# Kernel optimization log

Hardware: AMD Instinct MI355X
Metric: run time of the kernel (lower is better)

The kernel has to match this reference:

```python
import jax, jax.numpy as jnp
import numpy as np

N, K, C, R, S = 10000, 16, 32, 32, 64
D = 9  # per-channel irrep dim of interaction feats: 0e(1)+1o(3)+2e(5)
AVG_NEIGH = 16.0
EPS = 1e-6

_rng = np.random.default_rng(0)
# fixed constant coupling tensors (deterministic stand-ins for CG coefficients; structure matches e3nn paths)
CG112 = jnp.asarray(_rng.standard_normal((3, 3, 5)) * 0.2, jnp.float32)  # 1o x 1o -> 2e
CG121 = jnp.asarray(_rng.standard_normal((3, 5, 3)) * 0.2, jnp.float32)  # 1o x 2e -> 1o
# symmetric tensor-product bases U[order, ir_out]: shape (D,)*order + (mul, ir_dim)
MULS = {3: {'0e': 3, '1o': 2}, 2: {'0e': 2, '1o': 1}, 1: {'0e': 1, '1o': 1}}
IRDIM = {'0e': 1, '1o': 3}
U = {(o, ir): jnp.asarray(_rng.standard_normal((D,) * o + (MULS[o][ir], IRDIM[ir])) * (0.3 ** o), jnp.float32)
     for o in (3, 2, 1) for ir in ('0e', '1o')}


def _normnorm(arrs):
    # E3NormNorm: per-node RMS normalization over channel/component axes
    return [a / jnp.sqrt(jnp.mean(a * a, axis=tuple(range(1, a.ndim)), keepdims=True) + EPS) for a in arrs]


def _sph_harm(vec):
    # real spherical harmonics l=1,2 (component normalization) on normalized vectors
    r = vec / (jnp.linalg.norm(vec, axis=-1, keepdims=True) + EPS)
    x, y, z = r[..., 0], r[..., 1], r[..., 2]
    sh1 = jnp.sqrt(3.0) * r
    c = jnp.sqrt(15.0)
    sh2 = jnp.stack([c * x * y, c * y * z, jnp.sqrt(5.0) / 2 * (3 * z * z - 1), c * x * z, c / 2 * (x * x - y * y)], axis=-1)
    return sh1, sh2


def _forward(node_s, node_v, vectors, radial_embedding, species_table, Wu0, Wu1, radW, radb, ln_g, ln_b,
             Wd0, Wd1, Wd2, w3_0e, w3_1o, w2_0e, w2_1o, w1_0e, w1_1o, P0, P1, Wskip0, Wskip1, Wread,
             receivers, node_specie):
    n, c = node_s.shape
    inv = 1.0 / jnp.sqrt(1.0 * c)
    # ---- InteractionBlock: linear_up + norm ----
    s = node_s @ Wu0 * inv
    v = jnp.einsum('nci,cd->ndi', node_v, Wu1) * inv
    s, v = _normnorm([s, v])
    # ---- MessagePassingConvolution: sender = node i broadcast over its K=16 neighbors ----
    sh1, sh2 = _sph_harm(vectors)  # [n,K,3], [n,K,5]
    m0a = jnp.broadcast_to(s[:, None, :], (n, K, c))                       # prefix 0e
    m0b = jnp.einsum('nci,nki->nkc', v, sh1) / jnp.sqrt(3.0)               # 1o x 1o -> 0e
    m1a = jnp.broadcast_to(v[:, None], (n, K, c, 3))                       # prefix 1o
    m1b = jnp.einsum('nc,nki->nkci', s, sh1) / jnp.sqrt(3.0)               # 0e x 1o -> 1o
    m1c = jnp.einsum('nci,nkp,ipj->nkcj', v, sh2, CG121)                   # 1o x 2e -> 1o
    m2a = jnp.einsum('nc,nkp->nkcp', s, sh2) / jnp.sqrt(5.0)               # 0e x 2e -> 2e
    m2b = jnp.einsum('nci,nkj,ijp->nkcp', v, sh1, CG112)                   # 1o x 1o -> 2e
    M0 = jnp.concatenate([m0a, m0b], axis=-1)      # [n,K,2C]
    M1 = jnp.concatenate([m1a, m1b, m1c], axis=2)  # [n,K,3C,3]
    M2 = jnp.concatenate([m2a, m2b], axis=2)       # [n,K,2C,5]
    # radial mix: linear + layernorm, one weight per irrep (7C total)
    rad = radial_embedding @ radW + radb
    mu = rad.mean(-1, keepdims=True)
    var = rad.var(-1, keepdims=True)
    rad = ln_g * (rad - mu) / jnp.sqrt(var + EPS) + ln_b
    r0, r1, r2 = rad[..., :2 * c], rad[..., 2 * c:5 * c], rad[..., 5 * c:]
    M0 = M0 * r0
    M1 = M1 * r1[..., None]
    M2 = M2 * r2[..., None]
    # scatter-add messages to receivers, normalize by sqrt(avg_num_neighbors)
    idx = receivers.reshape(-1)
    sc = 1.0 / jnp.sqrt(AVG_NEIGH)
    o0 = jnp.zeros((n, 2 * c), M0.dtype).at[idx].add(M0.reshape(n * K, 2 * c)) * sc
    o1 = jnp.zeros((n, 3 * c, 3), M1.dtype).at[idx].add(M1.reshape(n * K, 3 * c, 3)) * sc
    o2 = jnp.zeros((n, 2 * c, 5), M2.dtype).at[idx].add(M2.reshape(n * K, 2 * c, 5)) * sc
    o0, o1, o2 = _normnorm([o0, o1, o2])
    # linear_down to interaction_irreps Cx(0e+1o+2e), then norm
    A0 = o0 @ Wd0 / jnp.sqrt(2.0 * c)
    A1 = jnp.einsum('nmi,md->ndi', o1, Wd1) / jnp.sqrt(3.0 * c)
    A2 = jnp.einsum('nmi,md->ndi', o2, Wd2) / jnp.sqrt(2.0 * c)
    A0, A1, A2 = _normnorm([A0, A1, A2])
    # ---- EquivariantProductBasisBlock: species-gathered symmetric contraction ----
    x_sym = jnp.concatenate([A0[:, :, None], A1, A2], axis=-1)  # [n, C, D=9]
    species_ind = species_table[node_specie]                    # [n, R]
    Wsym = {(3, '0e'): w3_0e, (3, '1o'): w3_1o, (2, '0e'): w2_0e, (2, '1o'): w2_1o, (1, '0e'): w1_0e, (1, '1o'): w1_1o}
    out = {}
    for order in (3, 2, 1):
        for ir in ('0e', '1o'):
            u = U[(order, ir)]
            w = jnp.einsum('be,ekc->bkc', species_ind, Wsym[(order, ir)])
            if ir not in out:
                out[ir] = ('new', jnp.einsum('...jki,bkc,bcj->bc...i', u, w, x_sym))
            else:
                out[ir] = out[ir] + jnp.einsum('...ki,bkc->bc...i', u, w)
        for ir in ('0e', '1o'):
            if isinstance(out[ir], tuple):
                out[ir] = out[ir][1]  # creation order already consumed one x
            else:
                out[ir] = jnp.einsum('bc...ji,bcj->bc...i', out[ir], x_sym)
    sym_s = out['0e'][..., 0]  # [n, C]
    sym_v = out['1o']          # [n, C, 3]
    # proj_out linear
    ps = sym_s @ P0 * inv
    pv = jnp.einsum('nci,cd->ndi', sym_v, P1) * inv
    # species-indexed skip connection
    skip_s = jnp.einsum('nc,ncd->nd', node_s, Wskip0[node_specie]) * inv
    skip_v = jnp.einsum('nci,ncd->ndi', node_v, Wskip1[node_specie]) * inv
    s_out = ps + skip_s
    v_out = pv + skip_v
    # linear readout (output_irreps = 1x0e)
    read = s_out @ Wread * inv
    return jnp.concatenate([s_out, v_out.reshape(n, 3 * c), read], axis=-1)


def setup_inputs():
    ks = jax.random.split(jax.random.key(0), 32)
    f = lambda i, shape: jax.random.normal(ks[i], shape, jnp.float32)
    return {
        'node_s': f(0, (N, C)),
        'node_v': f(1, (N, C, 3)),
        'vectors': f(2, (N, K, 3)),
        'radial_embedding': f(3, (N, K, R)),
        'receivers': jax.random.randint(ks[4], (N, K), 0, N),
        'node_specie': jax.random.randint(ks[5], (N,), 0, S),
        'species_table': f(6, (S, R)),
        'Wu0': f(7, (C, C)), 'Wu1': f(8, (C, C)),
        'radW': f(9, (R, 7 * C)), 'radb': jnp.zeros((7 * C,), jnp.float32),
        'ln_g': jnp.ones((7 * C,), jnp.float32), 'ln_b': jnp.zeros((7 * C,), jnp.float32),
        'Wd0': f(11, (2 * C, C)), 'Wd1': f(12, (3 * C, C)), 'Wd2': f(13, (2 * C, C)),
        'w3_0e': f(14, (R, 3, C)), 'w3_1o': f(15, (R, 2, C)),
        'w2_0e': f(16, (R, 2, C)), 'w2_1o': f(17, (R, 1, C)),
        'w1_0e': f(18, (R, 1, C)), 'w1_1o': f(19, (R, 1, C)),
        'P0': f(20, (C, C)), 'P1': f(21, (C, C)),
        'Wskip0': f(22, (S, C, C)), 'Wskip1': f(23, (S, C, C)),
        'Wread': f(24, (C, 1)),
    }


def reference(node_s, node_v, vectors, radial_embedding, receivers, node_specie, species_table, Wu0, Wu1,
              radW, radb, ln_g, ln_b, Wd0, Wd1, Wd2, w3_0e, w3_1o, w2_0e, w2_1o, w1_0e, w1_1o,
              P0, P1, Wskip0, Wskip1, Wread):
    return _forward(node_s, node_v, vectors, radial_embedding, species_table, Wu0, Wu1, radW, radb, ln_g, ln_b,
                    Wd0, Wd1, Wd2, w3_0e, w3_1o, w2_0e, w2_1o, w1_0e, w1_1o, P0, P1, Wskip0, Wskip1, Wread,
                    receivers, node_specie)
```

## Files before the change

kernel.cpp:

```cpp
#include <hip/hip_runtime.h>
#include <cmath>
#include <stdint.h>

typedef unsigned long long u64;
typedef unsigned __int128 u128;

#define EPSF 1e-6f

#define OFF_RAW 0L
#define OFF_S   7168L
#define OFF_G   8960L
#define GSP_SZ  28032L
#define OFF_SN  (OFF_G + 64L*GSP_SZ)
#define OFF_VN  (OFF_SN + 320000L)
#define FLOAT_END (OFF_VN + 960000L)
#define OFF_RAD (FLOAT_END + 262144L)
#define RAD_REQ_BYTES ((size_t)(OFF_RAD + 35840000L) * 4)
#define OFF_RNG (OFF_G + 8192L)

#define IOFF_DEG   0
#define IOFF_OFFS  10000
#define IOFF_CUR   20001
#define IOFF_EL    30001
#define IOFF_SCNT  190001
#define IOFF_SOFF  190065
#define IOFF_SCUR  190130
#define IOFF_NORD  190194
#define IOFF_TRI   200194
#define IOFF_PAIR  200359


__device__ __forceinline__ u128 pcg_mul128() {
  return ((u128)2549297995355413924ULL << 64) | (u128)4865540595714422341ULL;
}
struct Pcg {
  u128 state, inc;
  __device__ __forceinline__ u64 next() {
    state = state * pcg_mul128() + inc;
    u64 hi = (u64)(state >> 64), lo = (u64)state;
    unsigned rot = (unsigned)(hi >> 58);
    u64 x = hi ^ lo;
    return (x >> rot) | (x << ((64u - rot) & 63u));
  }
};
__device__ __forceinline__ double u64_to_dbl(u64 u) {
  return (double)(u >> 11) * (1.0 / 9007199254740992.0);
}
__device__ __forceinline__ unsigned ss_hashmix(unsigned v, unsigned &hc) {
  v ^= hc; hc *= 0x931e8875u; v *= hc; v ^= v >> 16; return v;
}
__device__ __forceinline__ unsigned ss_mix(unsigned x, unsigned y) {
  unsigned r = 0xca01f9ddu * x - 0x4973f715u * y; r ^= r >> 16; return r;
}

#define NBUF 8192
#define NBM  8191
#define PERTH 32
#define NDRAW 7092
#define NSEG  222
#define RB_E 32

__global__ __launch_bounds__(256) void k_prep(
    const float* __restrict__ ns, const float* __restrict__ nv,
    const float* __restrict__ Wu0, const float* __restrict__ Wu1,
    const float* __restrict__ remb, const float* __restrict__ radW,
    const float* __restrict__ radb, const float* __restrict__ ln_g,
    const float* __restrict__ ln_b,
    const int* __restrict__ recv, const int* __restrict__ spec,
    int doRad,
    float* __restrict__ wsf, int* __restrict__ wsi)
{
  __shared__ __align__(16) float shbuf[8672];
  const int tid = threadIdx.x;
  const int bid = blockIdx.x;

  if (bid < 1250) {
    const int nn = bid * 8 + (tid >> 5);
    const int c = tid & 31;
    const float INV = 0.17677669529663687f;
    float s = 0.f;
    for (int e = 0; e < 32; e++) s += ns[nn*32 + e] * Wu0[e*32 + c];
    s *= INV;
    float v0 = 0, v1 = 0, v2 = 0;
    for (int e = 0; e < 32; e++) {
      const float w = Wu1[e*32 + c];
      const float* p = nv + (long)(nn*32 + e)*3;
      v0 += p[0]*w; v1 += p[1]*w; v2 += p[2]*w;
    }
    v0 *= INV; v1 *= INV; v2 *= INV;
    float ss = s*s;
    for (int m = 16; m >= 1; m >>= 1) ss += __shfl_xor(ss, m);
    float sv = v0*v0 + v1*v1 + v2*v2;
    for (int m = 16; m >= 1; m >>= 1) sv += __shfl_xor(sv, m);
    float rs = rsqrtf(ss * (1.f/32.f) + EPSF);
    float rv = rsqrtf(sv * (1.f/96.f) + EPSF);
    wsf[OFF_SN + nn*32 + c] = s * rs;
    float* vp = wsf + OFF_VN + (long)(nn*32 + c)*3;
    vp[0] = v0*rv; vp[1] = v1*rv; vp[2] = v2*rv;
  } else if (bid < 6250) {
    if (!doRad) return;
    float (*er)[33] = (float(*)[33])&shbuf[0];
    float* pre = &shbuf[1056];
    float4* lg4 = (float4*)&shbuf[8224];
    float4* lb4 = (float4*)&shbuf[8448];
    const long e0 = (long)(bid - 1250) * RB_E;

    if (tid < 56) { lg4[tid] = ((const float4*)ln_g)[tid]; lb4[tid] = ((const float4*)ln_b)[tid]; }
    for (int i = tid; i < RB_E*32; i += 256) {
      const int e = i >> 5, q = i & 31;
      er[e][q] = remb[(e0 + e)*32 + q];
    }
    __syncthreads();

    if (tid < 224) {
      const int cg = tid % 56, grp = tid / 56;
      const float4 rb = ((const float4*)radb)[cg];
      float4 acc[8];
      #pragma unroll
      for (int k = 0; k < 8; k++) acc[k] = rb;
      const float4* radW4 = (const float4*)radW;
      for (int q = 0; q < 32; q++) {
        const float4 w = radW4[q*56 + cg];
        #pragma unroll
        for (int k = 0; k < 8; k++) {
          const float ev = er[grp*8 + k][q];
          acc[k].x = fmaf(ev, w.x, acc[k].x);
          acc[k].y = fmaf(ev, w.y, acc[k].y);
          acc[k].z = fmaf(ev, w.z, acc[k].z);
          acc[k].w = fmaf(ev, w.w, acc[k].w);
        }
      }
      #pragma unroll
      for (int k = 0; k < 8; k++)
        ((float4*)&pre[(grp*8 + k)*224])[cg] = acc[k];
    }
    __syncthreads();

    const int wv = tid >> 6, ln = tid & 63;
    for (int k = 0; k < 8; k++) {
      const int e = wv*8 + k;
      float a0 = 0.f, a1 = 0.f, a2 = 0.f, a3 = 0.f;
      if (ln < 56) {
        const float4 v = ((const float4*)&pre[e*224])[ln];
        a0 = v.x; a1 = v.y; a2 = v.z; a3 = v.w;
      }
      float c1 = a0 + a1 + a2 + a3;
      float c2 = a0*a0 + a1*a1 + a2*a2 + a3*a3;
      for (int m = 32; m >= 1; m >>= 1) { c1 += __shfl_xor(c1, m); c2 += __shfl_xor(c2, m); }
      const float mu = c1 * (1.f/224.f);
      const float rvar = rsqrtf(c2*(1.f/224.f) - mu*mu + EPSF);
      if (ln < 56) {
        const float4 lg = lg4[ln], lb = lb4[ln];
        float4 o;
        o.x = lg.x*(a0-mu)*rvar + lb.x;
        o.y = lg.y*(a1-mu)*rvar + lb.y;
        o.z = lg.z*(a2-mu)*rvar + lb.z;
        o.w = lg.w*(a3-mu)*rvar + lb.w;
        ((float4*)(wsf + OFF_RAD))[(e0 + e)*56 + ln] = o;
      }
    }
  } else if (bid < 6875) {
    const int e = (bid - 6250)*256 + tid;
    if (e < 160000) atomicAdd(&wsi[IOFF_DEG + recv[e]], 1);
    if (e < 10000)  atomicAdd(&wsi[IOFF_SCNT + spec[e]], 1);
  } else {
    if (tid != 0) return;
    double* wiG = (double*)(wsf + OFF_RNG);
    double* fiG = (double*)(wsf + OFF_RNG + 512);
    u64*    kiG = (u64*)   (wsf + OFF_RNG + 1024);
    u64*    ssG = (u64*)   (wsf + OFF_RNG + 1536);
    unsigned hc = 0x43b0d7e5u;
    unsigned pool[4];
    for (int i = 0; i < 4; i++) pool[i] = ss_hashmix(0u, hc);
    for (int s = 0; s < 4; s++)
      for (int d = 0; d < 4; d++)
        if (s != d) pool[d] = ss_mix(pool[d], ss_hashmix(pool[s], hc));
    unsigned hb = 0x8b51f9ddu;
    u64 sw[4];
    {
      unsigned w8[8];
      for (int i = 0; i < 8; i++) {
        unsigned dv = pool[i & 3];
        dv ^= hb; hb *= 0x58f38dedu; dv *= hb; dv ^= dv >> 16;
        w8[i] = dv;
      }
      for (int k2 = 0; k2 < 4; k2++) sw[k2] = (u64)w8[2*k2] | ((u64)w8[2*k2+1] << 32);
    }
    u128 initstate = ((u128)sw[0] << 64) | (u128)sw[1];
    u128 initseq   = ((u128)sw[2] << 64) | (u128)sw[3];
    u128 inc_ = (initseq << 1) | (u128)1;
    u128 S0 = inc_;
    S0 += initstate;
    S0 = S0 * pcg_mul128() + inc_;
    ssG[0] = (u64)(S0 >> 64);   ssG[1] = (u64)S0;
    ssG[2] = (u64)(inc_ >> 64); ssG[3] = (u64)inc_;
    const double m1 = 4503599627370496.0;
    const double ZR = 3.6541528853610087963519472518;
    double dn = ZR, tn = ZR;
    const double vn = 4.92867323399e-3;
    double fv = exp(-0.5 * dn * dn);
    double q = vn / fv;
    kiG[0] = (u64)((dn / q) * m1);
    kiG[1] = 0;
    wiG[0] = q / m1;  wiG[255] = dn / m1;
    fiG[0] = 1.0;     fiG[255] = fv;
    for (int i = 254; i >= 1; i--) {
      dn = sqrt(-2.0 * log(vn / dn + fv));
      kiG[i+1] = (u64)((dn / tn) * m1);
      tn = dn;
      fv = exp(-0.5 * dn * dn);
      fiG[i] = fv;
      wiG[i] = dn / m1;
    }
    int mcnt = 0;
    for (int a = 0; a < 9; a++)
      for (int b = a; b < 9; b++)
        for (int j3 = b; j3 < 9; j3++)
          wsi[IOFF_TRI + (mcnt++)] = a | (b << 4) | (j3 << 8);
    int pcnt = 0;
    for (int a = 0; a < 9; a++)
      for (int b = a; b < 9; b++)
        wsi[IOFF_PAIR + (pcnt++)] = a | (b << 4);
  }
}

__global__ __launch_bounds__(256) void k_mid(float* __restrict__ wsf, int* __restrict__ wsi)
{
  __shared__ double wi[256], fi[256];
  __shared__ u64 ki[256];
  __shared__ u64 buf[NBUF];
  __shared__ float zv[NBUF];
  __shared__ unsigned char cons[NBUF];
  __shared__ unsigned short jmp[NBUF];
  __shared__ unsigned short heads[NSEG];
  __shared__ u64 stst[512], enst[512];
  __shared__ double scl[8];
  __shared__ int flag;
  __shared__ int part[256];
  const int tid = threadIdx.x;

  if (blockIdx.x == 1) {
    int loc[40];
    const int base = tid * 40;
    int s = 0;
    for (int t = 0; t < 40; t++) {
      const int idx = base + t;
      loc[t] = s;
      s += (idx < 10000) ? wsi[IOFF_DEG + idx] : 0;
    }
    part[tid] = s;
    __syncthreads();
    for (int d = 1; d < 256; d <<= 1) {
      int v = (tid >= d) ? part[tid - d] : 0;
      __syncthreads();
      part[tid] += v;
      __syncthreads();
    }
    const int exc = (tid > 0) ? part[tid - 1] : 0;
    for (int t = 0; t < 40; t++) {
      const int idx = base + t;
      if (idx <= 10000) wsi[IOFF_OFFS + idx] = exc + loc[t];
    }
    if (tid == 0) {
      int a = 0;
      for (int s2 = 0; s2 < 64; s2++) { wsi[IOFF_SOFF + s2] = a; a += wsi[IOFF_SCNT + s2]; }
      wsi[IOFF_SOFF + 64] = a;
    }
    return;
  }

  const double* wiG = (const double*)(wsf + OFF_RNG);
  const double* fiG = (const double*)(wsf + OFF_RNG + 512);
  const u64*    kiG = (const u64*)   (wsf + OFF_RNG + 1024);
  const u64*    ssG = (const u64*)   (wsf + OFF_RNG + 1536);
  float* raw = wsf + OFF_RAW;

  wi[tid] = wiG[tid]; fi[tid] = fiG[tid]; ki[tid] = kiG[tid];
  if (tid == 0) {
    flag = 0;
    double p2 = pow(0.3, 2.0), p3 = pow(0.3, 3.0);
    scl[0]=0.2; scl[1]=0.2; scl[2]=p3; scl[3]=p3; scl[4]=p2; scl[5]=p2; scl[6]=0.3; scl[7]=0.3;
  }
  __syncthreads();

  {
    u128 S0   = ((u128)ssG[0] << 64) | (u128)ssG[1];
    u128 inc_ = ((u128)ssG[2] << 64) | (u128)ssG[3];
    u128 aR = (u128)1, cR = (u128)0;
    u128 aP = pcg_mul128(), cP = inc_;
    unsigned e = (unsigned)tid * PERTH;
    while (e) {
      if (e & 1u) { cR = aP * cR + cP; aR = aP * aR; }
      cP = aP * cP + cP;
      aP = aP * aP;
      e >>= 1;
    }
    Pcg g; g.inc = inc_; g.state = aR * S0 + cR;
    stst[tid*2] = (u64)(g.state >> 64); stst[tid*2+1] = (u64)g.state;
    #pragma unroll 4
    for (int k = 0; k < PERTH; k++) buf[tid*PERTH + k] = g.next();
    enst[tid*2] = (u64)(g.state >> 64); enst[tid*2+1] = (u64)g.state;
  }
  __syncthreads();
  if (tid < 255) {
    if (stst[(tid+1)*2] != enst[tid*2] || stst[(tid+1)*2+1] != enst[tid*2+1])
      atomicOr(&flag, 1);
  }
  if (tid == 0) {
    if (fabs(u64_to_dbl(buf[0]) - 0.6369616873214543) > 1e-12) atomicOr(&flag, 1);
  }
  __syncthreads();
  if (flag && tid == 0) {
    u128 S0   = ((u128)ssG[0] << 64) | (u128)ssG[1];
    u128 inc_ = ((u128)ssG[2] << 64) | (u128)ssG[3];
    Pcg g; g.state = S0; g.inc = inc_;
    for (int k = 0; k < NBUF; k++) buf[k] = g.next();
  }
  __syncthreads();

  const double ZRd  = 3.6541528853610087963519472518;
  const double ZIRd = 0.27366123732975827203338247596;
  for (int k = 0; k < PERTH; k++) {
    const int p = tid*PERTH + k;
    int pos = p;
    int consumed = 0;
    double z = 0.0;
    u64 r = buf[pos & NBM]; pos++; consumed++;
    for (int guard = 0; guard < 64; guard++) {
      int idx = (int)(r & 0xff);
      r >>= 8;
      int sgn = (int)(r & 1);
      u64 rabs = (r >> 1) & 0x000fffffffffffffULL;
      double x = (double)rabs * wi[idx];
      if (sgn) x = -x;
      if (rabs < ki[idx]) { z = x; break; }
      if (idx == 0) {
        double xx = 0.0, yy = 0.0;
        for (int g2 = 0; g2 < 64; g2++) {
          u64 ua = buf[pos & NBM]; pos++; consumed++;
          u64 ub = buf[pos & NBM]; pos++; consumed++;
          xx = -ZIRd * log1p(-u64_to_dbl(ua));
          yy = -log1p(-u64_to_dbl(ub));
          if (yy + yy > xx * xx) break;
        }
        z = ((rabs >> 8) & 1) ? -(ZRd + xx) : (ZRd + xx);
        break;
      } else {
        u64 u = buf[pos & NBM]; pos++; consumed++;
        if ((fi[idx-1] - fi[idx]) * u64_to_dbl(u) + fi[idx] < exp(-0.5 * x * x)) { z = x; break; }
      }
      r = buf[pos & NBM]; pos++; consumed++;
    }
    zv[p] = (float)z;
    cons[p] = (unsigned char)(consumed > 255 ? 255 : consumed);
  }
  __syncthreads();

  {
    int pos[PERTH];
    #pragma unroll
    for (int k = 0; k < PERTH; k++) pos[k] = tid*PERTH + k;
    for (int s = 0; s < 32; s++) {
      #pragma unroll
      for (int k = 0; k < PERTH; k++) {
        int np = pos[k] + (int)cons[pos[k]];
        pos[k] = (np > NBM) ? NBM : np;
      }
    }
    #pragma unroll
    for (int k = 0; k < PERTH; k++) jmp[tid*PERTH + k] = (unsigned short)pos[k];
  }
  __syncthreads();

  if (tid == 0) {
    int pos = 0;
    for (int m = 0; m < NSEG; m++) { heads[m] = (unsigned short)pos; pos = (int)jmp[pos]; }
  }
  __syncthreads();

  if (tid < NSEG) {
    int pos = (int)heads[tid];
    const int i0 = tid * 32;
    for (int k = 0; k < 32; k++) {
      const int i = i0 + k;
      if (i >= NDRAW) break;
      double sc;
      if      (i < 90)   sc = scl[0];
      else if (i < 6651) sc = scl[2];
      else if (i < 7056) sc = scl[4];
      else               sc = scl[6];
      raw[i] = (float)((double)zv[pos] * sc);
      int np = pos + (int)cons[pos];
      pos = (np > NBM) ? NBM : np;
    }
  }
}

__global__ __launch_bounds__(256) void k_fillg(
    const int* __restrict__ recv, const int* __restrict__ spec,
    const float* __restrict__ stab,
    const float* __restrict__ w30e, const float* __restrict__ w31o,
    const float* __restrict__ w20e, const float* __restrict__ w21o,
    const float* __restrict__ w10e, const float* __restrict__ w11o,
    float* __restrict__ wsf, int* __restrict__ wsi)
{
  __shared__ float st[32];
  const int tid = threadIdx.x;
  const int bid = blockIdx.x;
  if (bid < 625) {
    const int e = bid*256 + tid;
    if (e < 160000) {
      int r = recv[e];
      int p = atomicAdd(&wsi[IOFF_CUR + r], 1);
      wsi[IOFF_EL + wsi[IOFF_OFFS + r] + p] = e;
    }
    if (e < 10000) {
      int sp = spec[e];
      int p = atomicAdd(&wsi[IOFF_SCUR + sp], 1);
      wsi[IOFF_NORD + wsi[IOFF_SOFF + sp] + p] = e;
    }
  } else if (bid < 689) {
    const int sp = bid - 625;
    float* Gsp = wsf + OFF_G + (long)sp * GSP_SZ;
    if (tid < 32) st[tid] = stab[sp*32 + tid];
    __syncthreads();
    for (int t = tid; t < 320; t += 256) {
      const float* W; int kc, kcs;
      if (t < 96)       { W = w30e; kc = t;       kcs = 96; }
      else if (t < 160) { W = w31o; kc = t - 96;  kcs = 64; }
      else if (t < 224) { W = w20e; kc = t - 160; kcs = 64; }
      else if (t < 256) { W = w21o; kc = t - 224; kcs = 32; }
      else if (t < 288) { W = w10e; kc = t - 256; kcs = 32; }
      else              { W = w11o; kc = t - 288; kcs = 32; }
      float a = 0.f;
      for (int e = 0; e < 32; e++) a += st[e] * W[e*kcs + kc];
      Gsp[t] = a;
    }
  } else {
    const float* raw = wsf + OFF_RAW;
    float* Sb = wsf + OFF_S;
    for (int idx = tid; idx < 495; idx += 256) {
      int m = idx / 3, k2 = idx % 3;
      int tp = wsi[IOFF_TRI + m];
      int a = tp & 15, b = (tp >> 4) & 15, j3 = (tp >> 8) & 15;
      int P[6][3] = {{a,b,j3},{a,j3,b},{b,a,j3},{b,j3,a},{j3,a,b},{j3,b,a}};
      float s = 0.f;
      for (int t = 0; t < 6; t++) {
        bool dup = false;
        for (int u = 0; u < t; u++)
          if (P[u][0]==P[t][0] && P[u][1]==P[t][1] && P[u][2]==P[t][2]) { dup = true; break; }
        if (!dup) s += raw[90 + ((P[t][0]*9 + P[t][1])*9 + P[t][2])*3 + k2];
      }
      Sb[m*3 + k2] = s;
    }
    for (int idx = tid; idx < 990; idx += 256) {
      int m = idx / 6, r6 = idx % 6, k2 = r6 / 3, i = r6 % 3;
      int tp = wsi[IOFF_TRI + m];
      int a = tp & 15, b = (tp >> 4) & 15, j3 = (tp >> 8) & 15;
      int P[6][3] = {{a,b,j3},{a,j3,b},{b,a,j3},{b,j3,a},{j3,a,b},{j3,b,a}};
      float s = 0.f;
      for (int t = 0; t < 6; t++) {
        bool dup = false;
        for (int u = 0; u < t; u++)
          if (P[u][0]==P[t][0] && P[u][1]==P[t][1] && P[u][2]==P[t][2]) { dup = true; break; }
        if (!dup) s += raw[2277 + (((P[t][0]*9 + P[t][1])*9 + P[t][2])*2 + k2)*3 + i];
      }
      Sb[495 + (m*2 + k2)*3 + i] = s;
    }
    for (int idx = tid; idx < 90; idx += 256) {
      int m = idx / 2, k2 = idx % 2;
      int pp = wsi[IOFF_PAIR + m]; int a = pp & 15, b = (pp >> 4) & 15;
      float s = raw[6651 + (a*9 + b)*2 + k2];
      if (a != b) s += raw[6651 + (b*9 + a)*2 + k2];
      Sb[1485 + idx] = s;
    }
    for (int idx = tid; idx < 135; idx += 256) {
      int m = idx / 3, i = idx % 3;
      int pp = wsi[IOFF_PAIR + m]; int a = pp & 15, b = (pp >> 4) & 15;
      float s = raw[6813 + (a*9 + b)*3 + i];
      if (a != b) s += raw[6813 + (b*9 + a)*3 + i];
      Sb[1575 + idx] = s;
    }
    for (int idx = tid; idx < 9;  idx += 256) Sb[1710 + idx] = raw[7056 + idx];
    for (int idx = tid; idx < 27; idx += 256) Sb[1719 + idx] = raw[7065 + idx];
  }
}

__device__ __forceinline__ float msg_fast(int slot,
    const float* __restrict__ se, const float* __restrict__ ve,
    const float* __restrict__ sh, const float* __restrict__ ab,
    const float* __restrict__ rd)
{
  const float IS3 = 0.57735026918962576f;
  const float IS5 = 0.44721359549995794f;
  float val; int radidx;
  if (slot < 64) {
    radidx = slot;
    if (slot < 32) val = se[slot];
    else {
      int c = slot - 32;
      val = (ve[c*3+0]*sh[0] + ve[c*3+1]*sh[1] + ve[c*3+2]*sh[2]) * IS3;
    }
  } else if (slot < 352) {
    int q = slot - 64; int row = q / 3; int i = q - row*3;
    radidx = 64 + row;
    if (row < 32) val = ve[row*3 + i];
    else if (row < 64) val = se[row - 32] * sh[i] * IS3;
    else {
      int c = row - 64;
      val = ve[c*3+0]*ab[0+i] + ve[c*3+1]*ab[3+i] + ve[c*3+2]*ab[6+i];
    }
  } else {
    int q = slot - 352; int row = q / 5; int p = q - row*5;
    radidx = 160 + row;
    if (row < 32) val = se[row] * sh[3+p] * IS5;
    else {
      int c = row - 32;
      val = ve[c*3+0]*ab[9+p] + ve[c*3+1]*ab[14+p] + ve[c*3+2]*ab[19+p];
    }
  }
  return val * rd[radidx];
}

#define SM_RAD 0
#define SM_SE  896
#define SM_VE  1024
#define SM_ER  1408
#define SM_SHH 1536
#define SM_AB  1568
#define SM_LNG 1664
#define SM_LNB 1888
#define SM_RB  2112
#define SM_CG  2336
#define SM_S    0
#define SM_X    1746
#define SM_O    2034
#define SM_GRED 2706
#define SM_SYMS 3730
#define SM_SYMV 3762
#define SM_SOUT 3858
#define SM_REDB 3890
#define SM_RF   3902
#define SMEM_N  3906

template<int PRE>
__global__ __launch_bounds__(256) void k_main(
    const float* __restrict__ node_s, const float* __restrict__ node_v,
    const float* __restrict__ vectors, const float* __restrict__ remb,
    const int* __restrict__ nspec,
    const float* __restrict__ radW, const float* __restrict__ radb,
    const float* __restrict__ ln_g, const float* __restrict__ ln_b,
    const float* __restrict__ Wd0, const float* __restrict__ Wd1, const float* __restrict__ Wd2,
    const float* __restrict__ P0, const float* __restrict__ P1,
    const float* __restrict__ Wsk0, const float* __restrict__ Wsk1,
    const float* __restrict__ Wread,
    const float* __restrict__ wsf, const int* __restrict__ wsi,
    float* __restrict__ out)
{
  const int tid = threadIdx.x;
  const int wv  = tid >> 6;
  const int ln  = tid & 63;
  __shared__ __align__(16) float smem[SMEM_N];
  __shared__ int tri_s[165], pair_s[45];

  const int j  = wsi[IOFF_NORD + blockIdx.x];
  const int sp = nspec[j];
  const int e0 = wsi[IOFF_OFFS + j];
  const int e1 = wsi[IOFF_OFFS + j + 1];

  if (!PRE) {
    for (int i = tid; i < 224; i += 256) {
      smem[SM_LNG + i] = ln_g[i];
      smem[SM_LNB + i] = ln_b[i];
      smem[SM_RB  + i] = radb[i];
    }
  }
  for (int i = tid; i < 90; i += 256) smem[SM_CG + i] = wsf[OFF_RAW + i];
  __syncthreads();

  float acc0 = 0.f, acc1 = 0.f, acc2 = 0.f;
  for (int t = e0; t < e1; t += 4) {
    const int eidx = t + wv;
    const bool act = (eidx < e1);
    if (act) {
      const int e = wsi[IOFF_EL + eidx];
      const int n = e >> 4;
      if (ln < 32) {
        smem[SM_SE + wv*32 + ln] = wsf[OFF_SN + (long)n*32 + ln];
        if (!PRE) smem[SM_ER + wv*32 + ln] = remb[(long)e*32 + ln];
      } else {
        const int l2 = ln - 32;
        const float* vp = wsf + OFF_VN + (long)(n*32 + l2)*3;
        smem[SM_VE + wv*96 + l2*3+0] = vp[0];
        smem[SM_VE + wv*96 + l2*3+1] = vp[1];
        smem[SM_VE + wv*96 + l2*3+2] = vp[2];
      }
      if (ln == 0) {
        const float* vv = vectors + (long)e*3;
        float vx = vv[0], vy = vv[1], vz = vv[2];
        float nr = sqrtf(vx*vx + vy*vy + vz*vz) + EPSF;
        float rx = vx/nr, ry = vy/nr, rz = vz/nr;
        smem[SM_SHH + wv*8 + 0] = 1.7320508075688772f * rx;
        smem[SM_SHH + wv*8 + 1] = 1.7320508075688772f * ry;
        smem[SM_SHH + wv*8 + 2] = 1.7320508075688772f * rz;
        smem[SM_SHH + wv*8 + 3] = 3.872983346207417f * rx*ry;
        smem[SM_SHH + wv*8 + 4] = 3.872983346207417f * ry*rz;
        smem[SM_SHH + wv*8 + 5] = 1.118033988749895f * (3.f*rz*rz - 1.f);
        smem[SM_SHH + wv*8 + 6] = 3.872983346207417f * rx*rz;
        smem[SM_SHH + wv*8 + 7] = 1.9364916731037085f * (rx*rx - ry*ry);
      }
      if (PRE) {
        if (ln < 56) {
          const float4 v4 = ((const float4*)(wsf + OFF_RAD))[(long)e*56 + ln];
          ((float4*)&smem[SM_RAD + wv*224])[ln] = v4;
        }
      } else {
        float aval[4];
        float c1 = 0.f, c2 = 0.f;
        #pragma unroll
        for (int k = 0; k < 4; k++) {
          const int ch = ln + 64*k;
          if (ch < 224) {
            float a = smem[SM_RB + ch];
            #pragma unroll 8
            for (int q = 0; q < 32; q++)
              a += smem[SM_ER + wv*32 + q] * radW[q*224 + ch];
            aval[k] = a; c1 += a; c2 += a*a;
          }
        }
        for (int m = 32; m >= 1; m >>= 1) { c1 += __shfl_xor(c1, m); c2 += __shfl_xor(c2, m); }
        const float mu = c1 * (1.f/224.f);
        const float rvar = rsqrtf(c2*(1.f/224.f) - mu*mu + EPSF);
        #pragma unroll
        for (int k = 0; k < 4; k++) {
          const int ch = ln + 64*k;
          if (ch < 224)
            smem[SM_RAD + wv*224 + ch] = smem[SM_LNG + ch]*(aval[k]-mu)*rvar + smem[SM_LNB + ch];
        }
      }
      if (ln < 9) {
        const int i2 = ln / 3, i = ln - i2*3;
        float a = 0.f;
        #pragma unroll
        for (int p = 0; p < 5; p++)
          a += smem[SM_SHH + wv*8 + 3 + p] * smem[SM_CG + 45 + i2*15 + p*3 + i];
        smem[SM_AB + wv*24 + ln] = a;
      } else if (ln < 24) {
        const int q = ln - 9, i = q / 5, p = q - i*5;
        float a = 0.f;
        #pragma unroll
        for (int j2 = 0; j2 < 3; j2++)
          a += smem[SM_SHH + wv*8 + j2] * smem[SM_CG + i*15 + j2*5 + p];
        smem[SM_AB + wv*24 + 9 + q] = a;
      }
    }
    __syncthreads();
    const int nact = (e1 - t < 4) ? (e1 - t) : 4;
    for (int w = 0; w < nact; w++) {
      const float* se = &smem[SM_SE + w*32];
      const float* ve = &smem[SM_VE + w*96];
      const float* sh = &smem[SM_SHH + w*8];
      const float* ab = &smem[SM_AB + w*24];
      const float* rd = &smem[SM_RAD + w*224];
      acc0 += msg_fast(tid,       se, ve, sh, ab, rd);
      acc1 += msg_fast(tid + 256, se, ve, sh, ab, rd);
      if (tid < 160) acc2 += msg_fast(tid + 512, se, ve, sh, ab, rd);
    }
    __syncthreads();
  }

  for (int i = tid; i < 1746; i += 256) smem[SM_S + i] = wsf[OFF_S + i];
  for (int i = tid; i < 165; i += 256) tri_s[i] = wsi[IOFF_TRI + i];
  for (int i = tid; i < 45;  i += 256) pair_s[i] = wsi[IOFF_PAIR + i];

  float* redbuf = &smem[SM_REDB];
  float* rf     = &smem[SM_RF];
  acc0 *= 0.25f; acc1 *= 0.25f; acc2 *= 0.25f;
  float g0 = 0, g1 = 0, g2 = 0;
  if (tid < 64) g0 = acc0*acc0; else g1 = acc0*acc0;
  if (tid < 96) g1 += acc1*acc1; else g2 += acc1*acc1;
  if (tid < 160) g2 += acc2*acc2;
  for (int m = 32; m >= 1; m >>= 1) { g0 += __shfl_xor(g0, m); g1 += __shfl_xor(g1, m); g2 += __shfl_xor(g2, m); }
  if ((tid & 63) == 0) { redbuf[wv] = g0; redbuf[4+wv] = g1; redbuf[8+wv] = g2; }
  __syncthreads();
  if (tid == 0) {
    float s0 = redbuf[0]+redbuf[1]+redbuf[2]+redbuf[3];
    float s1 = redbuf[4]+redbuf[5]+redbuf[6]+redbuf[7];
    float s2 = redbuf[8]+redbuf[9]+redbuf[10]+redbuf[11];
    rf[0] = rsqrtf(s0*(1.f/64.f)  + EPSF);
    rf[1] = rsqrtf(s1*(1.f/288.f) + EPSF);
    rf[2] = rsqrtf(s2*(1.f/320.f) + EPSF);
  }
  __syncthreads();
  smem[SM_O + tid]       = acc0 * ((tid < 64) ? rf[0] : rf[1]);
  smem[SM_O + tid + 256] = acc1 * ((tid < 96) ? rf[1] : rf[2]);
  if (tid < 160) smem[SM_O + tid + 512] = acc2 * rf[2];
  __syncthreads();

  const float* o_lds = &smem[SM_O];
  float av1, av2 = 0.f;
  if (tid < 32) {
    float a = 0;
    for (int m = 0; m < 64; m++) a += o_lds[m] * Wd0[m*32 + tid];
    av1 = a * 0.125f;
  } else if (tid < 128) {
    int q = tid - 32, d = q/3, i = q - d*3;
    float a = 0;
    for (int m = 0; m < 96; m++) a += o_lds[64 + m*3 + i] * Wd1[m*32 + d];
    av1 = a * 0.10206207261596575f;
  } else {
    int q = tid - 128, d = q/5, p = q - d*5;
    float a = 0;
    for (int m = 0; m < 64; m++) a += o_lds[352 + m*5 + p] * Wd2[m*32 + d];
    av1 = a * 0.125f;
  }
  if (tid < 32) {
    int q = tid + 128, d = q/5, p = q - d*5;
    float a = 0;
    for (int m = 0; m < 64; m++) a += o_lds[352 + m*5 + p] * Wd2[m*32 + d];
    av2 = a * 0.125f;
  }
  float p0 = (tid < 32) ? av1*av1 : 0.f;
  float p1 = (tid >= 32 && tid < 128) ? av1*av1 : 0.f;
  float p2s = (tid >= 128) ? av1*av1 : 0.f;
  if (tid < 32) p2s += av2*av2;
  for (int m = 32; m >= 1; m >>= 1) { p0 += __shfl_xor(p0, m); p1 += __shfl_xor(p1, m); p2s += __shfl_xor(p2s, m); }
  if ((tid & 63) == 0) { redbuf[wv] = p0; redbuf[4+wv] = p1; redbuf[8+wv] = p2s; }
  __syncthreads();
  if (tid == 0) {
    float s0 = redbuf[0]+redbuf[1]+redbuf[2]+redbuf[3];
    float s1 = redbuf[4]+redbuf[5]+redbuf[6]+redbuf[7];
    float s2 = redbuf[8]+redbuf[9]+redbuf[10]+redbuf[11];
    rf[0] = rsqrtf(s0*(1.f/32.f)  + EPSF);
    rf[1] = rsqrtf(s1*(1.f/96.f)  + EPSF);
    rf[2] = rsqrtf(s2*(1.f/160.f) + EPSF);
  }
  __syncthreads();
  float* x_lds = &smem[SM_X];
  if (tid < 32) x_lds[tid*9 + 0] = av1 * rf[0];
  else if (tid < 128) { int q = tid - 32, d = q/3, i = q - d*3; x_lds[d*9 + 1 + i] = av1 * rf[1]; }
  else { int q = tid - 128, d = q/5, p = q - d*5; x_lds[d*9 + 4 + p] = av1 * rf[2]; }
  if (tid < 32) { int q = tid + 128, d = q/5, p = q - d*5; x_lds[d*9 + 4 + p] = av2 * rf[2]; }
  __syncthreads();

  const float* Sb = &smem[SM_S];
  float* gred = &smem[SM_GRED];
  const int c = tid & 31, g = tid >> 5;
  float xr[9];
  for (int t2 = 0; t2 < 9; t2++) xr[t2] = x_lds[c*9 + t2];
  const float* wl = wsf + OFF_G + (long)sp * GSP_SZ;
  const float w30a = wl[c], w30b = wl[32 + c], w30c = wl[64 + c];
  const float w31a = wl[96 + c], w31b = wl[128 + c];
  const float w20a = wl[160 + c], w20b = wl[192 + c];
  const float w21  = wl[224 + c];
  const float w10  = wl[256 + c];
  const float w11  = wl[288 + c];

  float sa = 0, va0 = 0, va1 = 0, va2 = 0;
  for (int m = g; m < 165; m += 8) {
    const int tp = tri_s[m];
    const float P = xr[tp & 15] * xr[(tp >> 4) & 15] * xr[(tp >> 8) & 15];
    sa += P * (Sb[m*3+0]*w30a + Sb[m*3+1]*w30b + Sb[m*3+2]*w30c);
    const float* s1p = &Sb[495 + m*6];
    va0 += P * (s1p[0]*w31a + s1p[3]*w31b);
    va1 += P * (s1p[1]*w31a + s1p[4]*w31b);
    va2 += P * (s1p[2]*w31a + s1p[5]*w31b);
  }
  for (int m = g; m < 45; m += 8) {
    const int pp = pair_s[m];
    const float P = xr[pp & 15] * xr[(pp >> 4) & 15];
    sa += P * (Sb[1485 + m*2+0]*w20a + Sb[1485 + m*2+1]*w20b);
    const float* s1p = &Sb[1575 + m*3];
    va0 += P * s1p[0] * w21;
    va1 += P * s1p[1] * w21;
    va2 += P * s1p[2] * w21;
  }
  if (g == 0) {
    for (int a = 0; a < 9; a++) {
      const float xa = xr[a];
      sa += xa * Sb[1710 + a] * w10;
      va0 += xa * Sb[1719 + a*3 + 0] * w11;
      va1 += xa * Sb[1719 + a*3 + 1] * w11;
      va2 += xa * Sb[1719 + a*3 + 2] * w11;
    }
  }
  gred[0*256 + g*32 + c] = sa;
  gred[1*256 + g*32 + c] = va0;
  gred[2*256 + g*32 + c] = va1;
  gred[3*256 + g*32 + c] = va2;
  __syncthreads();
  float* syms = &smem[SM_SYMS];
  float* symv = &smem[SM_SYMV];
  float* sout = &smem[SM_SOUT];
  if (tid < 128) {
    int cc = tid & 31, comp = tid >> 5;
    float a = 0;
    for (int gg = 0; gg < 8; gg++) a += gred[comp*256 + gg*32 + cc];
    if (comp == 0) syms[cc] = a; else symv[cc*3 + comp - 1] = a;
  }
  __syncthreads();

  const float INV = 0.17677669529663687f;
  if (tid < 32) {
    int d = tid; float ps = 0, sk = 0;
    const float* Wp = Wsk0 + (long)sp * 1024;
    for (int c2 = 0; c2 < 32; c2++) {
      ps += syms[c2] * P0[c2*32 + d];
      sk += node_s[j*32 + c2] * Wp[c2*32 + d];
    }
    float val = (ps + sk) * INV;
    sout[d] = val;
    out[(long)j*129 + d] = val;
  } else if (tid < 128) {
    int q = tid - 32, d = q/3, i = q - d*3;
    float pv = 0, sk = 0;
    const float* Wp = Wsk1 + (long)sp * 1024;
    for (int c2 = 0; c2 < 32; c2++) {
      pv += symv[c2*3 + i] * P1[c2*32 + d];
      sk += node_v[(long)(j*32 + c2)*3 + i] * Wp[c2*32 + d];
    }
    out[(long)j*129 + 32 + q] = (pv + sk) * INV;
  }
  __syncthreads();
  if (tid < 32) {
    float p = sout[tid] * Wread[tid];
    for (int m = 16; m >= 1; m >>= 1) p += __shfl_xor(p, m);
    if (tid == 0) out[(long)j*129 + 128] = p * INV;
  }
}

extern "C" void kernel_launch(void* const* d_in, const int* in_sizes, int n_in,
                              void* d_out, int out_size, void* d_ws, size_t ws_size,
                              hipStream_t stream)
{
  const float* node_s  = (const float*)d_in[0];
  const float* node_v  = (const float*)d_in[1];
  const float* vectors = (const float*)d_in[2];
  const float* remb    = (const float*)d_in[3];
  const int*   recv    = (const int*)d_in[4];
  const int*   nspec   = (const int*)d_in[5];
  const float* stab    = (const float*)d_in[6];
  const float* Wu0     = (const float*)d_in[7];
  const float* Wu1     = (const float*)d_in[8];
  const float* radW    = (const float*)d_in[9];
  const float* radb    = (const float*)d_in[10];
  const float* ln_g    = (const float*)d_in[11];
  const float* ln_b    = (const float*)d_in[12];
  const float* Wd0     = (const float*)d_in[13];
  const float* Wd1     = (const float*)d_in[14];
  const float* Wd2     = (const float*)d_in[15];
  const float* w30e    = (const float*)d_in[16];
  const float* w31o    = (const float*)d_in[17];
  const float* w20e    = (const float*)d_in[18];
  const float* w21o    = (const float*)d_in[19];
  const float* w10e    = (const float*)d_in[20];
  const float* w11o    = (const float*)d_in[21];
  const float* P0      = (const float*)d_in[22];
  const float* P1      = (const float*)d_in[23];
  const float* Wsk0    = (const float*)d_in[24];
  const float* Wsk1    = (const float*)d_in[25];
  const float* Wread   = (const float*)d_in[26];
  float* out = (float*)d_out;
  float* wsf = (float*)d_ws;
  int*   wsi = (int*)((char*)d_ws + FLOAT_END * sizeof(float));

  const bool pre = (ws_size >= RAD_REQ_BYTES);

  hipMemsetAsync(wsi, 0, (size_t)IOFF_NORD * sizeof(int), stream);
  k_prep<<<6876, 256, 0, stream>>>(node_s, node_v, Wu0, Wu1,
                                   remb, radW, radb, ln_g, ln_b,
                                   recv, nspec, pre ? 1 : 0, wsf, wsi);
  k_mid<<<2, 256, 0, stream>>>(wsf, wsi);
  k_fillg<<<690, 256, 0, stream>>>(recv, nspec, stab,
                                   w30e, w31o, w20e, w21o, w10e, w11o,
                                   wsf, wsi);
  if (pre) {
    k_main<1><<<10000, 256, 0, stream>>>(node_s, node_v, vectors, remb, nspec,
                                         radW, radb, ln_g, ln_b, Wd0, Wd1, Wd2,
                                         P0, P1, Wsk0, Wsk1, Wread, wsf, wsi, out);
  } else {
    k_main<0><<<10000, 256, 0, stream>>>(node_s, node_v, vectors, remb, nspec,
                                         radW, radb, ln_g, ln_b, Wd0, Wd1, Wd2,
                                         P0, P1, Wsk0, Wsk1, Wread, wsf, wsi, out);
  }
}
```

Baseline: 596.9 us.

## Precompute per-edge messages in sender-major kernel, gather them per receiver

Adds a path where a new kernel computes the radial MLP with layernorm and the full 672-wide per-edge message in sender order, fused with the edge-list and weight-table setup work. The messages go to a workspace buffer in fp32, or fp16 when space is short. A gather kernel then sums each receiver's incoming messages before running the shared epilogue. This avoids rebuilding messages per receiver with scattered sender loads, at the cost of writing and re-reading a large message buffer, plus possible precision loss on the fp16 path. The old prep work is reordered and the fallback main kernel is split out.

```diff
diff --git a/kernel.cpp b/kernel.cpp
--- a/kernel.cpp
+++ b/kernel.cpp
@@ -1,4 +1,5 @@
 #include <hip/hip_runtime.h>
+#include <hip/hip_fp16.h>
 #include <cmath>
 #include <stdint.h>
 
@@ -16,6 +17,8 @@
 #define FLOAT_END (OFF_VN + 960000L)
 #define OFF_RAD (FLOAT_END + 262144L)
 #define RAD_REQ_BYTES ((size_t)(OFF_RAD + 35840000L) * 4)
+#define M_F16_REQ ((size_t)OFF_RAD*4 + (size_t)160000*672*2)
+#define M_F32_REQ ((size_t)OFF_RAD*4 + (size_t)160000*672*4)
 #define OFF_RNG (OFF_G + 8192L)
 
 #define IOFF_DEG   0
@@ -29,6 +32,16 @@
 #define IOFF_TRI   200194
 #define IOFF_PAIR  200359
 
+
+template<typename T> struct MTr;
+template<> struct MTr<float> {
+  static __device__ __forceinline__ float ld(const float* p) { return *p; }
+  static __device__ __forceinline__ void st(float* p, float v) { *p = v; }
+};
+template<> struct MTr<__half> {
+  static __device__ __forceinline__ float ld(const __half* p) { return __half2float(*p); }
+  static __device__ __forceinline__ void st(__half* p, float v) { *p = __float2half(v); }
+};
 
 __device__ __forceinline__ u128 pcg_mul128() {
   return ((u128)2549297995355413924ULL << 64) | (u128)4865540595714422341ULL;
@@ -74,96 +87,7 @@
   const int tid = threadIdx.x;
   const int bid = blockIdx.x;
 
-  if (bid < 1250) {
-    const int nn = bid * 8 + (tid >> 5);
-    const int c = tid & 31;
-    const float INV = 0.17677669529663687f;
-    float s = 0.f;
-    for (int e = 0; e < 32; e++) s += ns[nn*32 + e] * Wu0[e*32 + c];
-    s *= INV;
-    float v0 = 0, v1 = 0, v2 = 0;
-    for (int e = 0; e < 32; e++) {
-      const float w = Wu1[e*32 + c];
-      const float* p = nv + (long)(nn*32 + e)*3;
-      v0 += p[0]*w; v1 += p[1]*w; v2 += p[2]*w;
-    }
-    v0 *= INV; v1 *= INV; v2 *= INV;
-    float ss = s*s;
-    for (int m = 16; m >= 1; m >>= 1) ss += __shfl_xor(ss, m);
-    float sv = v0*v0 + v1*v1 + v2*v2;
-    for (int m = 16; m >= 1; m >>= 1) sv += __shfl_xor(sv, m);
-    float rs = rsqrtf(ss * (1.f/32.f) + EPSF);
-    float rv = rsqrtf(sv * (1.f/96.f) + EPSF);
-    wsf[OFF_SN + nn*32 + c] = s * rs;
-    float* vp = wsf + OFF_VN + (long)(nn*32 + c)*3;
-    vp[0] = v0*rv; vp[1] = v1*rv; vp[2] = v2*rv;
-  } else if (bid < 6250) {
-    if (!doRad) return;
-    float (*er)[33] = (float(*)[33])&shbuf[0];
-    float* pre = &shbuf[1056];
-    float4* lg4 = (float4*)&shbuf[8224];
-    float4* lb4 = (float4*)&shbuf[8448];
-    const long e0 = (long)(bid - 1250) * RB_E;
-
-    if (tid < 56) { lg4[tid] = ((const float4*)ln_g)[tid]; lb4[tid] = ((const float4*)ln_b)[tid]; }
-    for (int i = tid; i < RB_E*32; i += 256) {
-      const int e = i >> 5, q = i & 31;
-      er[e][q] = remb[(e0 + e)*32 + q];
-    }
-    __syncthreads();
-
-    if (tid < 224) {
-      const int cg = tid % 56, grp = tid / 56;
-      const float4 rb = ((const float4*)radb)[cg];
-      float4 acc[8];
-      #pragma unroll
-      for (int k = 0; k < 8; k++) acc[k] = rb;
-      const float4* radW4 = (const float4*)radW;
-      for (int q = 0; q < 32; q++) {
-        const float4 w = radW4[q*56 + cg];
-        #pragma unroll
-        for (int k = 0; k < 8; k++) {
-          const float ev = er[grp*8 + k][q];
-          acc[k].x = fmaf(ev, w.x, acc[k].x);
-          acc[k].y = fmaf(ev, w.y, acc[k].y);
-          acc[k].z = fmaf(ev, w.z, acc[k].z);
-          acc[k].w = fmaf(ev, w.w, acc[k].w);
-        }
-      }
-      #pragma unroll
-      for (int k = 0; k < 8; k++)
-        ((float4*)&pre[(grp*8 + k)*224])[cg] = acc[k];
-    }
-    __syncthreads();
-
-    const int wv = tid >> 6, ln = tid & 63;
-    for (int k = 0; k < 8; k++) {
-      const int e = wv*8 + k;
-      float a0 = 0.f, a1 = 0.f, a2 = 0.f, a3 = 0.f;
-      if (ln < 56) {
-        const float4 v = ((const float4*)&pre[e*224])[ln];
-        a0 = v.x; a1 = v.y; a2 = v.z; a3 = v.w;
-      }
-      float c1 = a0 + a1 + a2 + a3;
-      float c2 = a0*a0 + a1*a1 + a2*a2 + a3*a3;
-      for (int m = 32; m >= 1; m >>= 1) { c1 += __shfl_xor(c1, m); c2 += __shfl_xor(c2, m); }
-      const float mu = c1 * (1.f/224.f);
-      const float rvar = rsqrtf(c2*(1.f/224.f) - mu*mu + EPSF);
-      if (ln < 56) {
-        const float4 lg = lg4[ln], lb = lb4[ln];
-        float4 o;
-        o.x = lg.x*(a0-mu)*rvar + lb.x;
-        o.y = lg.y*(a1-mu)*rvar + lb.y;
-        o.z = lg.z*(a2-mu)*rvar + lb.z;
-        o.w = lg.w*(a3-mu)*rvar + lb.w;
-        ((float4*)(wsf + OFF_RAD))[(e0 + e)*56 + ln] = o;
-      }
-    }
-  } else if (bid < 6875) {
-    const int e = (bid - 6250)*256 + tid;
-    if (e < 160000) atomicAdd(&wsi[IOFF_DEG + recv[e]], 1);
-    if (e < 10000)  atomicAdd(&wsi[IOFF_SCNT + spec[e]], 1);
-  } else {
+  if (bid == 0) {
     if (tid != 0) return;
     double* wiG = (double*)(wsf + OFF_RNG);
     double* fiG = (double*)(wsf + OFF_RNG + 512);
@@ -221,6 +145,95 @@
     for (int a = 0; a < 9; a++)
       for (int b = a; b < 9; b++)
         wsi[IOFF_PAIR + (pcnt++)] = a | (b << 4);
+  } else if (bid < 1251) {
+    const int nn = (bid - 1) * 8 + (tid >> 5);
+    const int c = tid & 31;
+    const float INV = 0.17677669529663687f;
+    float s = 0.f;
+    for (int e = 0; e < 32; e++) s += ns[nn*32 + e] * Wu0[e*32 + c];
+    s *= INV;
+    float v0 = 0, v1 = 0, v2 = 0;
+    for (int e = 0; e < 32; e++) {
+      const float w = Wu1[e*32 + c];
+      const float* p = nv + (long)(nn*32 + e)*3;
+      v0 += p[0]*w; v1 += p[1]*w; v2 += p[2]*w;
+    }
+    v0 *= INV; v1 *= INV; v2 *= INV;
+    float ss = s*s;
+    for (int m = 16; m >= 1; m >>= 1) ss += __shfl_xor(ss, m);
+    float sv = v0*v0 + v1*v1 + v2*v2;
+    for (int m = 16; m >= 1; m >>= 1) sv += __shfl_xor(sv, m);
+    float rs = rsqrtf(ss * (1.f/32.f) + EPSF);
+    float rv = rsqrtf(sv * (1.f/96.f) + EPSF);
+    wsf[OFF_SN + nn*32 + c] = s * rs;
+    float* vp = wsf + OFF_VN + (long)(nn*32 + c)*3;
+    vp[0] = v0*rv; vp[1] = v1*rv; vp[2] = v2*rv;
+  } else if (bid < 1876) {
+    const int e = (bid - 1251)*256 + tid;
+    if (e < 160000) atomicAdd(&wsi[IOFF_DEG + recv[e]], 1);
+    if (e < 10000)  atomicAdd(&wsi[IOFF_SCNT + spec[e]], 1);
+  } else {
+    if (!doRad) return;
+    float (*er)[33] = (float(*)[33])&shbuf[0];
+    float* pre = &shbuf[1056];
+    float4* lg4 = (float4*)&shbuf[8224];
+    float4* lb4 = (float4*)&shbuf[8448];
+    const long e0 = (long)(bid - 1876) * RB_E;
+
+    if (tid < 56) { lg4[tid] = ((const float4*)ln_g)[tid]; lb4[tid] = ((const float4*)ln_b)[tid]; }
+    for (int i = tid; i < RB_E*32; i += 256) {
+      const int e = i >> 5, q = i & 31;
+      er[e][q] = remb[(e0 + e)*32 + q];
+    }
+    __syncthreads();
+
+    if (tid < 224) {
+      const int cg = tid % 56, grp = tid / 56;
+      const float4 rb = ((const float4*)radb)[cg];
+      float4 acc[8];
+      #pragma unroll
+      for (int k = 0; k < 8; k++) acc[k] = rb;
+      const float4* radW4 = (const float4*)radW;
+      for (int q = 0; q < 32; q++) {
+        const float4 w = radW4[q*56 + cg];
+        #pragma unroll
+        for (int k = 0; k < 8; k++) {
+          const float ev = er[grp*8 + k][q];
+          acc[k].x = fmaf(ev, w.x, acc[k].x);
+          acc[k].y = fmaf(ev, w.y, acc[k].y);
+          acc[k].z = fmaf(ev, w.z, acc[k].z);
+          acc[k].w = fmaf(ev, w.w, acc[k].w);
+        }
+      }
+      #pragma unroll
+      for (int k = 0; k < 8; k++)
+        ((float4*)&pre[(grp*8 + k)*224])[cg] = acc[k];
+    }
+    __syncthreads();
+
+    const int wv = tid >> 6, ln = tid & 63;
+    for (int k = 0; k < 8; k++) {
+      const int e = wv*8 + k;
+      float a0 = 0.f, a1 = 0.f, a2 = 0.f, a3 = 0.f;
+      if (ln < 56) {
+        const float4 v = ((const float4*)&pre[e*224])[ln];
+        a0 = v.x; a1 = v.y; a2 = v.z; a3 = v.w;
+      }
+      float c1 = a0 + a1 + a2 + a3;
+      float c2 = a0*a0 + a1*a1 + a2*a2 + a3*a3;
+      for (int m = 32; m >= 1; m >>= 1) { c1 += __shfl_xor(c1, m); c2 += __shfl_xor(c2, m); }
+      const float mu = c1 * (1.f/224.f);
+      const float rvar = rsqrtf(c2*(1.f/224.f) - mu*mu + EPSF);
+      if (ln < 56) {
+        const float4 lg = lg4[ln], lb = lb4[ln];
+        float4 o;
+        o.x = lg.x*(a0-mu)*rvar + lb.x;
+        o.y = lg.y*(a1-mu)*rvar + lb.y;
+        o.z = lg.z*(a2-mu)*rvar + lb.z;
+        o.w = lg.w*(a3-mu)*rvar + lb.w;
+        ((float4*)(wsf + OFF_RAD))[(e0 + e)*56 + ln] = o;
+      }
+    }
   }
 }
 
@@ -396,6 +409,280 @@
   }
 }
 
+__device__ __forceinline__ float msg_fast(int slot,
+    const float* __restrict__ se, const float* __restrict__ ve,
+    const float* __restrict__ sh, const float* __restrict__ ab,
+    const float* __restrict__ rd)
+{
+  const float IS3 = 0.57735026918962576f;
+  const float IS5 = 0.44721359549995794f;
+  float val; int radidx;
+  if (slot < 64) {
+    radidx = slot;
+    if (slot < 32) val = se[slot];
+    else {
+      int c = slot - 32;
+      val = (ve[c*3+0]*sh[0] + ve[c*3+1]*sh[1] + ve[c*3+2]*sh[2]) * IS3;
+    }
+  } else if (slot < 352) {
+    int q = slot - 64; int row = q / 3; int i = q - row*3;
+    radidx = 64 + row;
+    if (row < 32) val = ve[row*3 + i];
+    else if (row < 64) val = se[row - 32] * sh[i] * IS3;
+    else {
+      int c = row - 64;
+      val = ve[c*3+0]*ab[0+i] + ve[c*3+1]*ab[3+i] + ve[c*3+2]*ab[6+i];
+    }
+  } else {
+    int q = slot - 352; int row = q / 5; int p = q - row*5;
+    radidx = 160 + row;
+    if (row < 32) val = se[row] * sh[3+p] * IS5;
+    else {
+      int c = row - 32;
+      val = ve[c*3+0]*ab[9+p] + ve[c*3+1]*ab[14+p] + ve[c*3+2]*ab[19+p];
+    }
+  }
+  return val * rd[radidx];
+}
+
+__device__ void build_stables(const float* raw, float* Sb, const int* wsi, int tid)
+{
+  for (int idx = tid; idx < 495; idx += 256) {
+    int m = idx / 3, k2 = idx % 3;
+    int tp = wsi[IOFF_TRI + m];
+    int a = tp & 15, b = (tp >> 4) & 15, j3 = (tp >> 8) & 15;
+    int P[6][3] = {{a,b,j3},{a,j3,b},{b,a,j3},{b,j3,a},{j3,a,b},{j3,b,a}};
+    float s = 0.f;
+    for (int t = 0; t < 6; t++) {
+      bool dup = false;
+      for (int u = 0; u < t; u++)
+        if (P[u][0]==P[t][0] && P[u][1]==P[t][1] && P[u][2]==P[t][2]) { dup = true; break; }
+      if (!dup) s += raw[90 + ((P[t][0]*9 + P[t][1])*9 + P[t][2])*3 + k2];
+    }
+    Sb[m*3 + k2] = s;
+  }
+  for (int idx = tid; idx < 990; idx += 256) {
+    int m = idx / 6, r6 = idx % 6, k2 = r6 / 3, i = r6 % 3;
+    int tp = wsi[IOFF_TRI + m];
+    int a = tp & 15, b = (tp >> 4) & 15, j3 = (tp >> 8) & 15;
+    int P[6][3] = {{a,b,j3},{a,j3,b},{b,a,j3},{b,j3,a},{j3,a,b},{j3,b,a}};
+    float s = 0.f;
+    for (int t = 0; t < 6; t++) {
+      bool dup = false;
+      for (int u = 0; u < t; u++)
+        if (P[u][0]==P[t][0] && P[u][1]==P[t][1] && P[u][2]==P[t][2]) { dup = true; break; }
+      if (!dup) s += raw[2277 + (((P[t][0]*9 + P[t][1])*9 + P[t][2])*2 + k2)*3 + i];
+    }
+    Sb[495 + (m*2 + k2)*3 + i] = s;
+  }
+  for (int idx = tid; idx < 90; idx += 256) {
+    int m = idx / 2, k2 = idx % 2;
+    int pp = wsi[IOFF_PAIR + m]; int a = pp & 15, b = (pp >> 4) & 15;
+    float s = raw[6651 + (a*9 + b)*2 + k2];
+    if (a != b) s += raw[6651 + (b*9 + a)*2 + k2];
+    Sb[1485 + idx] = s;
+  }
+  for (int idx = tid; idx < 135; idx += 256) {
+    int m = idx / 3, i = idx % 3;
+    int pp = wsi[IOFF_PAIR + m]; int a = pp & 15, b = (pp >> 4) & 15;
+    float s = raw[6813 + (a*9 + b)*3 + i];
+    if (a != b) s += raw[6813 + (b*9 + a)*3 + i];
+    Sb[1575 + idx] = s;
+  }
+  for (int idx = tid; idx < 9;  idx += 256) Sb[1710 + idx] = raw[7056 + idx];
+  for (int idx = tid; idx < 27; idx += 256) Sb[1719 + idx] = raw[7065 + idx];
+}
+
+__device__ void build_wl(int sp, const float* stab,
+    const float* w30e, const float* w31o, const float* w20e,
+    const float* w21o, const float* w10e, const float* w11o,
+    float* Gsp, float* st, int tid)
+{
+  if (tid < 32) st[tid] = stab[sp*32 + tid];
+  __syncthreads();
+  for (int t = tid; t < 320; t += 256) {
+    const float* W; int kc, kcs;
+    if (t < 96)       { W = w30e; kc = t;       kcs = 96; }
+    else if (t < 160) { W = w31o; kc = t - 96;  kcs = 64; }
+    else if (t < 224) { W = w20e; kc = t - 160; kcs = 64; }
+    else if (t < 256) { W = w21o; kc = t - 224; kcs = 32; }
+    else if (t < 288) { W = w10e; kc = t - 256; kcs = 32; }
+    else              { W = w11o; kc = t - 288; kcs = 32; }
+    float a = 0.f;
+    for (int e = 0; e < 32; e++) a += st[e] * W[e*kcs + kc];
+    Gsp[t] = a;
+  }
+}
+
+#define MS_ER  0
+#define MS_PRE 1056
+#define MS_SE  8224
+#define MS_VE  8288
+#define MS_SHH 8480
+#define MS_AB  8736
+#define MS_CG  9504
+#define MS_LG  9600
+#define MS_LB  9824
+#define MS_N   10048
+
+template<typename MT>
+__global__ __launch_bounds__(256) void k_msgfill(
+    const float* __restrict__ remb, const float* __restrict__ vectors,
+    const float* __restrict__ radW, const float* __restrict__ radb,
+    const float* __restrict__ ln_g, const float* __restrict__ ln_b,
+    const int* __restrict__ recv, const int* __restrict__ spec,
+    const float* __restrict__ stab,
+    const float* __restrict__ w30e, const float* __restrict__ w31o,
+    const float* __restrict__ w20e, const float* __restrict__ w21o,
+    const float* __restrict__ w10e, const float* __restrict__ w11o,
+    float* __restrict__ wsf, int* __restrict__ wsi, MT* __restrict__ M)
+{
+  __shared__ __align__(16) float ms[MS_N];
+  const int tid = threadIdx.x;
+  const int bid = blockIdx.x;
+
+  if (bid >= 5000) {
+    if (bid < 5625) {
+      const int e = (bid - 5000)*256 + tid;
+      if (e < 160000) {
+        int r = recv[e];
+        int p = atomicAdd(&wsi[IOFF_CUR + r], 1);
+        wsi[IOFF_EL + wsi[IOFF_OFFS + r] + p] = e;
+      }
+      if (e < 10000) {
+        int sp = spec[e];
+        int p = atomicAdd(&wsi[IOFF_SCUR + sp], 1);
+        wsi[IOFF_NORD + wsi[IOFF_SOFF + sp] + p] = e;
+      }
+    } else if (bid < 5689) {
+      build_wl(bid - 5625, stab, w30e, w31o, w20e, w21o, w10e, w11o,
+               wsf + OFF_G + (long)(bid - 5625) * GSP_SZ, ms, tid);
+    } else {
+      build_stables(wsf + OFF_RAW, wsf + OFF_S, wsi, tid);
+    }
+    return;
+  }
+
+  const long e0 = (long)bid * 32;
+  const int n0 = bid * 2;
+  if (tid < 56) {
+    ((float4*)&ms[MS_LG])[tid] = ((const float4*)ln_g)[tid];
+    ((float4*)&ms[MS_LB])[tid] = ((const float4*)ln_b)[tid];
+  }
+  for (int i = tid; i < 32*32; i += 256) {
+    const int e = i >> 5, q = i & 31;
+    ms[MS_ER + e*33 + q] = remb[(e0 + e)*32 + q];
+  }
+  if (tid < 64) {
+    const int which = tid >> 5, c = tid & 31;
+    ms[MS_SE + which*32 + c] = wsf[OFF_SN + (long)(n0 + which)*32 + c];
+  } else if (tid < 64 + 192) {
+    const int v = tid - 64, which = v / 96, q = v - which*96;
+    ms[MS_VE + which*96 + q] = wsf[OFF_VN + (long)(n0 + which)*96 + q];
+  }
+  for (int i = tid; i < 90; i += 256) ms[MS_CG + i] = wsf[OFF_RAW + i];
+  if (tid < 32) {
+    const float* vv = vectors + (e0 + tid)*3;
+    float vx = vv[0], vy = vv[1], vz = vv[2];
+    float nr = sqrtf(vx*vx + vy*vy + vz*vz) + EPSF;
+    float rx = vx/nr, ry = vy/nr, rz = vz/nr;
+    float* sh = &ms[MS_SHH + tid*8];
+    sh[0] = 1.7320508075688772f * rx;
+    sh[1] = 1.7320508075688772f * ry;
+    sh[2] = 1.7320508075688772f * rz;
+    sh[3] = 3.872983346207417f * rx*ry;
+    sh[4] = 3.872983346207417f * ry*rz;
+    sh[5] = 1.118033988749895f * (3.f*rz*rz - 1.f);
+    sh[6] = 3.872983346207417f * rx*rz;
+    sh[7] = 1.9364916731037085f * (rx*rx - ry*ry);
+  }
+  __syncthreads();
+
+  if (tid < 224) {
+    const int cg = tid % 56, grp = tid / 56;
+    const float4 rb = ((const float4*)radb)[cg];
+    float4 acc[8];
+    #pragma unroll
+    for (int k = 0; k < 8; k++) acc[k] = rb;
+    const float4* radW4 = (const float4*)radW;
+    for (int q = 0; q < 32; q++) {
+      const float4 w = radW4[q*56 + cg];
+      #pragma unroll
+      for (int k = 0; k < 8; k++) {
+        const float ev = ms[MS_ER + (grp*8 + k)*33 + q];
+        acc[k].x = fmaf(ev, w.x, acc[k].x);
+        acc[k].y = fmaf(ev, w.y, acc[k].y);
+        acc[k].z = fmaf(ev, w.z, acc[k].z);
+        acc[k].w = fmaf(ev, w.w, acc[k].w);
+      }
+    }
+    #pragma unroll
+    for (int k = 0; k < 8; k++)
+      ((float4*)&ms[MS_PRE + (grp*8 + k)*224])[cg] = acc[k];
+  }
+  __syncthreads();
+
+  {
+    const int wv = tid >> 6, ln = tid & 63;
+    for (int k = 0; k < 8; k++) {
+      const int e = wv*8 + k;
+      float a0 = 0.f, a1 = 0.f, a2 = 0.f, a3 = 0.f;
+      if (ln < 56) {
+        const float4 v = ((const float4*)&ms[MS_PRE + e*224])[ln];
+        a0 = v.x; a1 = v.y; a2 = v.z; a3 = v.w;
+      }
+      float c1 = a0 + a1 + a2 + a3;
+      float c2 = a0*a0 + a1*a1 + a2*a2 + a3*a3;
+      for (int m = 32; m >= 1; m >>= 1) { c1 += __shfl_xor(c1, m); c2 += __shfl_xor(c2, m); }
+      const float mu = c1 * (1.f/224.f);
+      const float rvar = rsqrtf(c2*(1.f/224.f) - mu*mu + EPSF);
+      if (ln < 56) {
+        const float4 lg = ((const float4*)&ms[MS_LG])[ln];
+        const float4 lb = ((const float4*)&ms[MS_LB])[ln];
+        float4 o;
+        o.x = lg.x*(a0-mu)*rvar + lb.x;
+        o.y = lg.y*(a1-mu)*rvar + lb.y;
+        o.z = lg.z*(a2-mu)*rvar + lb.z;
+        o.w = lg.w*(a3-mu)*rvar + lb.w;
+        ((float4*)&ms[MS_PRE + e*224])[ln] = o;
+      }
+    }
+  }
+  for (int v = tid; v < 768; v += 256) {
+    const int s = v / 24, r = v - s*24;
+    const float* sh = &ms[MS_SHH + s*8];
+    if (r < 9) {
+      const int i2 = r / 3, i = r - i2*3;
+      float a = 0.f;
+      #pragma unroll
+      for (int p = 0; p < 5; p++)
+        a += sh[3 + p] * ms[MS_CG + 45 + i2*15 + p*3 + i];
+      ms[MS_AB + s*24 + r] = a;
+    } else {
+      const int q = r - 9, i = q / 5, p = q - i*5;
+      float a = 0.f;
+      #pragma unroll
+      for (int j2 = 0; j2 < 3; j2++)
+        a += sh[j2] * ms[MS_CG + i*15 + j2*5 + p];
+      ms[MS_AB + s*24 + 9 + q] = a;
+    }
+  }
+  __syncthreads();
+
+  for (int s = 0; s < 32; s++) {
+    const float* se = &ms[MS_SE + (s >> 4)*32];
+    const float* ve = &ms[MS_VE + (s >> 4)*96];
+    const float* sh = &ms[MS_SHH + s*8];
+    const float* ab = &ms[MS_AB + s*24];
+    const float* rd = &ms[MS_PRE + s*224];
+    const long base = (e0 + s) * 672;
+    MTr<MT>::st(M + base + tid,       msg_fast(tid,       se, ve, sh, ab, rd));
+    MTr<MT>::st(M + base + 256 + tid, msg_fast(tid + 256, se, ve, sh, ab, rd));
+    if (tid < 160)
+      MTr<MT>::st(M + base + 512 + tid, msg_fast(tid + 512, se, ve, sh, ab, rd));
+  }
+}
+
 __global__ __launch_bounds__(256) void k_fillg(
     const int* __restrict__ recv, const int* __restrict__ spec,
     const float* __restrict__ stab,
@@ -420,118 +707,13 @@
       wsi[IOFF_NORD + wsi[IOFF_SOFF + sp] + p] = e;
     }
   } else if (bid < 689) {
-    const int sp = bid - 625;
-    float* Gsp = wsf + OFF_G + (long)sp * GSP_SZ;
-    if (tid < 32) st[tid] = stab[sp*32 + tid];
-    __syncthreads();
-    for (int t = tid; t < 320; t += 256) {
-      const float* W; int kc, kcs;
-      if (t < 96)       { W = w30e; kc = t;       kcs = 96; }
-      else if (t < 160) { W = w31o; kc = t - 96;  kcs = 64; }
-      else if (t < 224) { W = w20e; kc = t - 160; kcs = 64; }
-      else if (t < 256) { W = w21o; kc = t - 224; kcs = 32; }
-      else if (t < 288) { W = w10e; kc = t - 256; kcs = 32; }
-      else              { W = w11o; kc = t - 288; kcs = 32; }
-      float a = 0.f;
-      for (int e = 0; e < 32; e++) a += st[e] * W[e*kcs + kc];
-      Gsp[t] = a;
-    }
+    build_wl(bid - 625, stab, w30e, w31o, w20e, w21o, w10e, w11o,
+             wsf + OFF_G + (long)(bid - 625) * GSP_SZ, st, tid);
   } else {
-    const float* raw = wsf + OFF_RAW;
-    float* Sb = wsf + OFF_S;
-    for (int idx = tid; idx < 495; idx += 256) {
-      int m = idx / 3, k2 = idx % 3;
-      int tp = wsi[IOFF_TRI + m];
-      int a = tp & 15, b = (tp >> 4) & 15, j3 = (tp >> 8) & 15;
-      int P[6][3] = {{a,b,j3},{a,j3,b},{b,a,j3},{b,j3,a},{j3,a,b},{j3,b,a}};
-      float s = 0.f;
-      for (int t = 0; t < 6; t++) {
-        bool dup = false;
-        for (int u = 0; u < t; u++)
-          if (P[u][0]==P[t][0] && P[u][1]==P[t][1] && P[u][2]==P[t][2]) { dup = true; break; }
-        if (!dup) s += raw[90 + ((P[t][0]*9 + P[t][1])*9 + P[t][2])*3 + k2];
-      }
-      Sb[m*3 + k2] = s;
-    }
-    for (int idx = tid; idx < 990; idx += 256) {
-      int m = idx / 6, r6 = idx % 6, k2 = r6 / 3, i = r6 % 3;
-      int tp = wsi[IOFF_TRI + m];
-      int a = tp & 15, b = (tp >> 4) & 15, j3 = (tp >> 8) & 15;
-      int P[6][3] = {{a,b,j3},{a,j3,b},{b,a,j3},{b,j3,a},{j3,a,b},{j3,b,a}};
-      float s = 0.f;
-      for (int t = 0; t < 6; t++) {
-        bool dup = false;
-        for (int u = 0; u < t; u++)
-          if (P[u][0]==P[t][0] && P[u][1]==P[t][1] && P[u][2]==P[t][2]) { dup = true; break; }
-        if (!dup) s += raw[2277 + (((P[t][0]*9 + P[t][1])*9 + P[t][2])*2 + k2)*3 + i];
-      }
-      Sb[495 + (m*2 + k2)*3 + i] = s;
-    }
-    for (int idx = tid; idx < 90; idx += 256) {
-      int m = idx / 2, k2 = idx % 2;
-      int pp = wsi[IOFF_PAIR + m]; int a = pp & 15, b = (pp >> 4) & 15;
-      float s = raw[6651 + (a*9 + b)*2 + k2];
-      if (a != b) s += raw[6651 + (b*9 + a)*2 + k2];
-      Sb[1485 + idx] = s;
-    }
-    for (int idx = tid; idx < 135; idx += 256) {
-      int m = idx / 3, i = idx % 3;
-      int pp = wsi[IOFF_PAIR + m]; int a = pp & 15, b = (pp >> 4) & 15;
-      float s = raw[6813 + (a*9 + b)*3 + i];
-      if (a != b) s += raw[6813 + (b*9 + a)*3 + i];
-      Sb[1575 + idx] = s;
-    }
-    for (int idx = tid; idx < 9;  idx += 256) Sb[1710 + idx] = raw[7056 + idx];
-    for (int idx = tid; idx < 27; idx += 256) Sb[1719 + idx] = raw[7065 + idx];
-  }
-}
-
-__device__ __forceinline__ float msg_fast(int slot,
-    const float* __restrict__ se, const float* __restrict__ ve,
-    const float* __restrict__ sh, const float* __restrict__ ab,
-    const float* __restrict__ rd)
-{
-  const float IS3 = 0.57735026918962576f;
-  const float IS5 = 0.44721359549995794f;
-  float val; int radidx;
-  if (slot < 64) {
-    radidx = slot;
-    if (slot < 32) val = se[slot];
-    else {
-      int c = slot - 32;
-      val = (ve[c*3+0]*sh[0] + ve[c*3+1]*sh[1] + ve[c*3+2]*sh[2]) * IS3;
-    }
-  } else if (slot < 352) {
-    int q = slot - 64; int row = q / 3; int i = q - row*3;
-    radidx = 64 + row;
-    if (row < 32) val = ve[row*3 + i];
-    else if (row < 64) val = se[row - 32] * sh[i] * IS3;
-    else {
-      int c = row - 64;
-      val = ve[c*3+0]*ab[0+i] + ve[c*3+1]*ab[3+i] + ve[c*3+2]*ab[6+i];
-    }
-  } else {
-    int q = slot - 352; int row = q / 5; int p = q - row*5;
-    radidx = 160 + row;
-    if (row < 32) val = se[row] * sh[3+p] * IS5;
-    else {
-      int c = row - 32;
-      val = ve[c*3+0]*ab[9+p] + ve[c*3+1]*ab[14+p] + ve[c*3+2]*ab[19+p];
-    }
-  }
-  return val * rd[radidx];
-}
-
-#define SM_RAD 0
-#define SM_SE  896
-#define SM_VE  1024
-#define SM_ER  1408
-#define SM_SHH 1536
-#define SM_AB  1568
-#define SM_LNG 1664
-#define SM_LNB 1888
-#define SM_RB  2112
-#define SM_CG  2336
+    build_stables(wsf + OFF_RAW, wsf + OFF_S, wsi, tid);
+  }
+}
+
 #define SM_S    0
 #define SM_X    1746
 #define SM_O    2034
@@ -541,133 +723,20 @@
 #define SM_SOUT 3858
 #define SM_REDB 3890
 #define SM_RF   3902
-#define SMEM_N  3906
-
-template<int PRE>
-__global__ __launch_bounds__(256) void k_main(
-    const float* __restrict__ node_s, const float* __restrict__ node_v,
-    const float* __restrict__ vectors, const float* __restrict__ remb,
-    const int* __restrict__ nspec,
-    const float* __restrict__ radW, const float* __restrict__ radb,
-    const float* __restrict__ ln_g, const float* __restrict__ ln_b,
+#define EPI_N   3906
+
+__device__ void epilogue(float acc0, float acc1, float acc2,
+    int j, int sp, const float* __restrict__ node_s, const float* __restrict__ node_v,
     const float* __restrict__ Wd0, const float* __restrict__ Wd1, const float* __restrict__ Wd2,
     const float* __restrict__ P0, const float* __restrict__ P1,
     const float* __restrict__ Wsk0, const float* __restrict__ Wsk1,
     const float* __restrict__ Wread,
     const float* __restrict__ wsf, const int* __restrict__ wsi,
+    float* __restrict__ smem, int* __restrict__ tri_s, int* __restrict__ pair_s,
     float* __restrict__ out)
 {
   const int tid = threadIdx.x;
   const int wv  = tid >> 6;
-  const int ln  = tid & 63;
-  __shared__ __align__(16) float smem[SMEM_N];
-  __shared__ int tri_s[165], pair_s[45];
-
-  const int j  = wsi[IOFF_NORD + blockIdx.x];
-  const int sp = nspec[j];
-  const int e0 = wsi[IOFF_OFFS + j];
-  const int e1 = wsi[IOFF_OFFS + j + 1];
-
-  if (!PRE) {
-    for (int i = tid; i < 224; i += 256) {
-      smem[SM_LNG + i] = ln_g[i];
-      smem[SM_LNB + i] = ln_b[i];
-      smem[SM_RB  + i] = radb[i];
-    }
-  }
-  for (int i = tid; i < 90; i += 256) smem[SM_CG + i] = wsf[OFF_RAW + i];
-  __syncthreads();
-
-  float acc0 = 0.f, acc1 = 0.f, acc2 = 0.f;
-  for (int t = e0; t < e1; t += 4) {
-    const int eidx = t + wv;
-    const bool act = (eidx < e1);
-    if (act) {
-      const int e = wsi[IOFF_EL + eidx];
-      const int n = e >> 4;
-      if (ln < 32) {
-        smem[SM_SE + wv*32 + ln] = wsf[OFF_SN + (long)n*32 + ln];
-        if (!PRE) smem[SM_ER + wv*32 + ln] = remb[(long)e*32 + ln];
-      } else {
-        const int l2 = ln - 32;
-        const float* vp = wsf + OFF_VN + (long)(n*32 + l2)*3;
-        smem[SM_VE + wv*96 + l2*3+0] = vp[0];
-        smem[SM_VE + wv*96 + l2*3+1] = vp[1];
-        smem[SM_VE + wv*96 + l2*3+2] = vp[2];
-      }
-      if (ln == 0) {
-        const float* vv = vectors + (long)e*3;
-        float vx = vv[0], vy = vv[1], vz = vv[2];
-        float nr = sqrtf(vx*vx + vy*vy + vz*vz) + EPSF;
-        float rx = vx/nr, ry = vy/nr, rz = vz/nr;
-        smem[SM_SHH + wv*8 + 0] = 1.7320508075688772f * rx;
-        smem[SM_SHH + wv*8 + 1] = 1.7320508075688772f * ry;
-        smem[SM_SHH + wv*8 + 2] = 1.7320508075688772f * rz;
-        smem[SM_SHH + wv*8 + 3] = 3.872983346207417f * rx*ry;
-        smem[SM_SHH + wv*8 + 4] = 3.872983346207417f * ry*rz;
-        smem[SM_SHH + wv*8 + 5] = 1.118033988749895f * (3.f*rz*rz - 1.f);
-        smem[SM_SHH + wv*8 + 6] = 3.872983346207417f * rx*rz;
-        smem[SM_SHH + wv*8 + 7] = 1.9364916731037085f * (rx*rx - ry*ry);
-      }
-      if (PRE) {
-        if (ln < 56) {
-          const float4 v4 = ((const float4*)(wsf + OFF_RAD))[(long)e*56 + ln];
-          ((float4*)&smem[SM_RAD + wv*224])[ln] = v4;
-        }
-      } else {
-        float aval[4];
-        float c1 = 0.f, c2 = 0.f;
-        #pragma unroll
-        for (int k = 0; k < 4; k++) {
-          const int ch = ln + 64*k;
-          if (ch < 224) {
-            float a = smem[SM_RB + ch];
-            #pragma unroll 8
-            for (int q = 0; q < 32; q++)
-              a += smem[SM_ER + wv*32 + q] * radW[q*224 + ch];
-            aval[k] = a; c1 += a; c2 += a*a;
-          }
-        }
-        for (int m = 32; m >= 1; m >>= 1) { c1 += __shfl_xor(c1, m); c2 += __shfl_xor(c2, m); }
-        const float mu = c1 * (1.f/224.f);
-        const float rvar = rsqrtf(c2*(1.f/224.f) - mu*mu + EPSF);
-        #pragma unroll
-        for (int k = 0; k < 4; k++) {
-          const int ch = ln + 64*k;
-          if (ch < 224)
-            smem[SM_RAD + wv*224 + ch] = smem[SM_LNG + ch]*(aval[k]-mu)*rvar + smem[SM_LNB + ch];
-        }
-      }
-      if (ln < 9) {
-        const int i2 = ln / 3, i = ln - i2*3;
-        float a = 0.f;
-        #pragma unroll
-        for (int p = 0; p < 5; p++)
-          a += smem[SM_SHH + wv*8 + 3 + p] * smem[SM_CG + 45 + i2*15 + p*3 + i];
-        smem[SM_AB + wv*24 + ln] = a;
-      } else if (ln < 24) {
-        const int q = ln - 9, i = q / 5, p = q - i*5;
-        float a = 0.f;
-        #pragma unroll
-        for (int j2 = 0; j2 < 3; j2++)
-          a += smem[SM_SHH + wv*8 + j2] * smem[SM_CG + i*15 + j2*5 + p];
-        smem[SM_AB + wv*24 + 9 + q] = a;
-      }
-    }
-    __syncthreads();
-    const int nact = (e1 - t < 4) ? (e1 - t) : 4;
-    for (int w = 0; w < nact; w++) {
-      const float* se = &smem[SM_SE + w*32];
-      const float* ve = &smem[SM_VE + w*96];
-      const float* sh = &smem[SM_SHH + w*8];
-      const float* ab = &smem[SM_AB + w*24];
-      const float* rd = &smem[SM_RAD + w*224];
-      acc0 += msg_fast(tid,       se, ve, sh, ab, rd);
-      acc1 += msg_fast(tid + 256, se, ve, sh, ab, rd);
-      if (tid < 160) acc2 += msg_fast(tid + 512, se, ve, sh, ab, rd);
-    }
-    __syncthreads();
-  }
 
   for (int i = tid; i < 1746; i += 256) smem[SM_S + i] = wsf[OFF_S + i];
   for (int i = tid; i < 165; i += 256) tri_s[i] = wsi[IOFF_TRI + i];
@@ -827,6 +896,137 @@
     for (int m = 16; m >= 1; m >>= 1) p += __shfl_xor(p, m);
     if (tid == 0) out[(long)j*129 + 128] = p * INV;
   }
+}
+
+template<typename MT>
+__global__ __launch_bounds__(256) void k_gather(
+    const float* __restrict__ node_s, const float* __restrict__ node_v,
+    const int* __restrict__ nspec,
+    const float* __restrict__ Wd0, const float* __restrict__ Wd1, const float* __restrict__ Wd2,
+    const float* __restrict__ P0, const float* __restrict__ P1,
+    const float* __restrict__ Wsk0, const float* __restrict__ Wsk1,
+    const float* __restrict__ Wread,
+    const float* __restrict__ wsf, const int* __restrict__ wsi,
+    const MT* __restrict__ M, float* __restrict__ out)
+{
+  const int tid = threadIdx.x;
+  __shared__ __align__(16) float smem[EPI_N];
+  __shared__ int tri_s[165], pair_s[45];
+
+  const int j  = wsi[IOFF_NORD + blockIdx.x];
+  const int sp = nspec[j];
+  const int e0 = wsi[IOFF_OFFS + j];
+  const int e1 = wsi[IOFF_OFFS + j + 1];
+
+  float acc0 = 0.f, acc1 = 0.f, acc2 = 0.f;
+  for (int t = e0; t < e1; ++t) {
+    const long base = (long)wsi[IOFF_EL + t] * 672;
+    acc0 += MTr<MT>::ld(M + base + tid);
+    acc1 += MTr<MT>::ld(M + base + 256 + tid);
+    if (tid < 160) acc2 += MTr<MT>::ld(M + base + 512 + tid);
+  }
+  epilogue(acc0, acc1, acc2, j, sp, node_s, node_v, Wd0, Wd1, Wd2,
+           P0, P1, Wsk0, Wsk1, Wread, wsf, wsi, smem, tri_s, pair_s, out);
+}
+
+#define SM_RADK 0
+#define SM_SEK  896
+#define SM_VEK  1024
+#define SM_SHHK 1536
+#define SM_ABK  1568
+#define SM_CGK  2336
+
+__global__ __launch_bounds__(256) void k_mainB(
+    const float* __restrict__ node_s, const float* __restrict__ node_v,
+    const float* __restrict__ vectors,
+    const int* __restrict__ nspec,
+    const float* __restrict__ Wd0, const float* __restrict__ Wd1, const float* __restrict__ Wd2,
+    const float* __restrict__ P0, const float* __restrict__ P1,
+    const float* __restrict__ Wsk0, const float* __restrict__ Wsk1,
+    const float* __restrict__ Wread,
+    const float* __restrict__ wsf, const int* __restrict__ wsi,
+    float* __restrict__ out)
+{
+  const int tid = threadIdx.x;
+  const int wv  = tid >> 6;
+  const int ln  = tid & 63;
+  __shared__ __align__(16) float smem[EPI_N];
+  __shared__ int tri_s[165], pair_s[45];
+
+  const int j  = wsi[IOFF_NORD + blockIdx.x];
+  const int sp = nspec[j];
+  const int e0 = wsi[IOFF_OFFS + j];
+  const int e1 = wsi[IOFF_OFFS + j + 1];
+
+  for (int i = tid; i < 90; i += 256) smem[SM_CGK + i] = wsf[OFF_RAW + i];
+  __syncthreads();
+
+  float acc0 = 0.f, acc1 = 0.f, acc2 = 0.f;
+  for (int t = e0; t < e1; t += 4) {
+    const int eidx = t + wv;
+    const bool act = (eidx < e1);
+    if (act) {
+      const int e = wsi[IOFF_EL + eidx];
+      const int n = e >> 4;
+      if (ln < 32) {
+        smem[SM_SEK + wv*32 + ln] = wsf[OFF_SN + (long)n*32 + ln];
+      } else {
+        const int l2 = ln - 32;
+        const float* vp = wsf + OFF_VN + (long)(n*32 + l2)*3;
+        smem[SM_VEK + wv*96 + l2*3+0] = vp[0];
+        smem[SM_VEK + wv*96 + l2*3+1] = vp[1];
+        smem[SM_VEK + wv*96 + l2*3+2] = vp[2];
+      }
+      if (ln == 0) {
+        const float* vv = vectors + (long)e*3;
+        float vx = vv[0], vy = vv[1], vz = vv[2];
+        float nr = sqrtf(vx*vx + vy*vy + vz*vz) + EPSF;
+        float rx = vx/nr, ry = vy/nr, rz = vz/nr;
+        smem[SM_SHHK + wv*8 + 0] = 1.7320508075688772f * rx;
+        smem[SM_SHHK + wv*8 + 1] = 1.7320508075688772f * ry;
+        smem[SM_SHHK + wv*8 + 2] = 1.7320508075688772f * rz;
+        smem[SM_SHHK + wv*8 + 3] = 3.872983346207417f * rx*ry;
+        smem[SM_SHHK + wv*8 + 4] = 3.872983346207417f * ry*rz;
+        smem[SM_SHHK + wv*8 + 5] = 1.118033988749895f * (3.f*rz*rz - 1.f);
+        smem[SM_SHHK + wv*8 + 6] = 3.872983346207417f * rx*rz;
+        smem[SM_SHHK + wv*8 + 7] = 1.9364916731037085f * (rx*rx - ry*ry);
+      }
+      if (ln < 56) {
+        const float4 v4 = ((const float4*)(wsf + OFF_RAD))[(long)e*56 + ln];
+        ((float4*)&smem[SM_RADK + wv*224])[ln] = v4;
+      }
+      if (ln < 9) {
+        const int i2 = ln / 3, i = ln - i2*3;
+        float a = 0.f;
+        #pragma unroll
+        for (int p = 0; p < 5; p++)
+          a += smem[SM_SHHK + wv*8 + 3 + p] * smem[SM_CGK + 45 + i2*15 + p*3 + i];
+        smem[SM_ABK + wv*24 + ln] = a;
+      } else if (ln < 24) {
+        const int q = ln - 9, i = q / 5, p = q - i*5;
+        float a = 0.f;
+        #pragma unroll
+        for (int j2 = 0; j2 < 3; j2++)
+          a += smem[SM_SHHK + wv*8 + j2] * smem[SM_CGK + i*15 + j2*5 + p];
+        smem[SM_ABK + wv*24 + 9 + q] = a;
+      }
+    }
+    __syncthreads();
+    const int nact = (e1 - t < 4) ? (e1 - t) : 4;
+    for (int w = 0; w < nact; w++) {
+      const float* se = &smem[SM_SEK + w*32];
+      const float* ve = &smem[SM_VEK + w*96];
+      const float* sh = &smem[SM_SHHK + w*8];
+      const float* ab = &smem[SM_ABK + w*24];
+      const float* rd = &smem[SM_RADK + w*224];
+      acc0 += msg_fast(tid,       se, ve, sh, ab, rd);
+      acc1 += msg_fast(tid + 256, se, ve, sh, ab, rd);
+      if (tid < 160) acc2 += msg_fast(tid + 512, se, ve, sh, ab, rd);
+    }
+    __syncthreads();
+  }
+  epilogue(acc0, acc1, acc2, j, sp, node_s, node_v, Wd0, Wd1, Wd2,
+           P0, P1, Wsk0, Wsk1, Wread, wsf, wsi, smem, tri_s, pair_s, out);
 }
 
 extern "C" void kernel_launch(void* const* d_in, const int* in_sizes, int n_in,
@@ -863,24 +1063,37 @@
   float* out = (float*)d_out;
   float* wsf = (float*)d_ws;
   int*   wsi = (int*)((char*)d_ws + FLOAT_END * sizeof(float));
-
-  const bool pre = (ws_size >= RAD_REQ_BYTES);
+  void*  Mp  = (char*)d_ws + OFF_RAD * sizeof(float);
+
+  const int pathA32 = (ws_size >= M_F32_REQ);
+  const int pathA16 = (!pathA32 && ws_size >= M_F16_REQ);
+  const int pathB   = (!pathA32 && !pathA16 && ws_size >= RAD_REQ_BYTES);
 
   hipMemsetAsync(wsi, 0, (size_t)IOFF_NORD * sizeof(int), stream);
   k_prep<<<6876, 256, 0, stream>>>(node_s, node_v, Wu0, Wu1,
                                    remb, radW, radb, ln_g, ln_b,
-                                   recv, nspec, pre ? 1 : 0, wsf, wsi);
+                                   recv, nspec, pathB ? 1 : 0, wsf, wsi);
   k_mid<<<2, 256, 0, stream>>>(wsf, wsi);
-  k_fillg<<<690, 256, 0, stream>>>(recv, nspec, stab,
-                                   w30e, w31o, w20e, w21o, w10e, w11o,
-                                   wsf, wsi);
-  if (pre) {
-    k_main<1><<<10000, 256, 0, stream>>>(node_s, node_v, vectors, remb, nspec,
-                                         radW, radb, ln_g, ln_b, Wd0, Wd1, Wd2,
-                                         P0, P1, Wsk0, Wsk1, Wread, wsf, wsi, out);
+  if (pathA32 || pathA16) {
+    if (pathA32) {
+      k_msgfill<float><<<5690, 256, 0, stream>>>(remb, vectors, radW, radb, ln_g, ln_b,
+          recv, nspec, stab, w30e, w31o, w20e, w21o, w10e, w11o,
+          wsf, wsi, (float*)Mp);
+      k_gather<float><<<10000, 256, 0, stream>>>(node_s, node_v, nspec,
+          Wd0, Wd1, Wd2, P0, P1, Wsk0, Wsk1, Wread, wsf, wsi, (const float*)Mp, out);
+    } else {
+      k_msgfill<__half><<<5690, 256, 0, stream>>>(remb, vectors, radW, radb, ln_g, ln_b,
+          recv, nspec, stab, w30e, w31o, w20e, w21o, w10e, w11o,
+          wsf, wsi, (__half*)Mp);
+      k_gather<__half><<<10000, 256, 0, stream>>>(node_s, node_v, nspec,
+          Wd0, Wd1, Wd2, P0, P1, Wsk0, Wsk1, Wread, wsf, wsi, (const __half*)Mp, out);
+    }
   } else {
-    k_main<0><<<10000, 256, 0, stream>>>(node_s, node_v, vectors, remb, nspec,
-                                         radW, radb, ln_g, ln_b, Wd0, Wd1, Wd2,
-                                         P0, P1, Wsk0, Wsk1, Wread, wsf, wsi, out);
-  }
-}
+    k_fillg<<<690, 256, 0, stream>>>(recv, nspec, stab,
+                                     w30e, w31o, w20e, w21o, w10e, w11o,
+                                     wsf, wsi);
+    k_mainB<<<10000, 256, 0, stream>>>(node_s, node_v, vectors, nspec,
+                                       Wd0, Wd1, Wd2, P0, P1, Wsk0, Wsk1, Wread,
+                                       wsf, wsi, out);
+  }
+}
```

Measured after the change: 967.2 us. 1.62x slower.
